# Performance work log

Measured on AMD Instinct MI355X. Metric: run time of the kernel, lower is better.

Reference implementation:

```python
import jax, jax.numpy as jnp
import numpy as np
import math

N_HEADS = 8
TANH_CLIP = 10.0
TEMP = 1.0


def setup_inputs() -> dict:
    key = jax.random.key(0)
    ks = jax.random.split(key, 8)
    B, N, D = 256, 2048, 128
    node_embeddings = jax.random.normal(ks[0], (B, N, D), dtype=jnp.float32)
    W_node = jax.random.normal(ks[1], (D, 3 * D), dtype=jnp.float32) / math.sqrt(D)
    W_fixed = jax.random.normal(ks[2], (D, D), dtype=jnp.float32) / math.sqrt(D)
    W_step = jax.random.normal(ks[3], (2 * D, D), dtype=jnp.float32) / math.sqrt(2 * D)
    W_out = jax.random.normal(ks[4], (D, D), dtype=jnp.float32) / math.sqrt(D)
    first_idx = jax.random.randint(ks[5], (B,), 0, N, dtype=jnp.int32)
    last_idx = jax.random.randint(ks[6], (B,), 0, N, dtype=jnp.int32)
    mask = jax.random.bernoulli(ks[7], 0.5, (B, N))
    mask = mask.at[:, 0].set(False)  # guarantee at least one feasible node per row
    return {"node_embeddings": node_embeddings, "W_node": W_node, "W_fixed": W_fixed,
            "W_step": W_step, "W_out": W_out, "first_idx": first_idx,
            "last_idx": last_idx, "mask": mask}


def reference(node_embeddings, W_node, W_fixed, W_step, W_out, first_idx, last_idx, mask):
    B, N, D = node_embeddings.shape
    H = N_HEADS
    hd = D // H  # key_dim = val_dim = embed_dim / n_heads
    neg_inf = -jnp.inf

    # --- _precompute ---
    graph_embed = node_embeddings.mean(axis=1)                # [B, D]
    fixed_context = graph_embed @ W_fixed                     # [B, D]
    proj = node_embeddings @ W_node                           # [B, N, 3D]
    gK, gV, logit_K = jnp.split(proj, 3, axis=-1)             # each [B, N, D]
    gK = gK.reshape(B, N, H, hd).transpose(2, 0, 1, 3)        # [H, B, N, hd]
    gV = gV.reshape(B, N, H, hd).transpose(2, 0, 1, 3)        # [H, B, N, hd]

    # --- step context: cat(first node emb, last node emb) ---
    first_emb = jnp.take_along_axis(node_embeddings, first_idx[:, None, None].astype(jnp.int32), axis=1)[:, 0]  # [B, D]
    last_emb = jnp.take_along_axis(node_embeddings, last_idx[:, None, None].astype(jnp.int32), axis=1)[:, 0]
    step_ctx = jnp.concatenate([first_emb, last_emb], axis=-1)  # [B, 2D]
    query = fixed_context + step_ctx @ W_step                 # [B, D]

    # --- glimpse multi-head attention (n_query = 1, masked inner) ---
    Q = query.reshape(B, H, hd).transpose(1, 0, 2)            # [H, B, hd]
    compat = jnp.einsum('hbd,hbnd->hbn', Q, gK) / math.sqrt(hd)  # [H, B, N]
    compat = jnp.where(mask[None, :, :], neg_inf, compat)     # mask_inner=True
    attn = jax.nn.softmax(compat, axis=-1)
    heads = jnp.einsum('hbn,hbnd->hbd', attn, gV)             # [H, B, hd]
    glimpse = heads.transpose(1, 0, 2).reshape(B, D) @ W_out  # project_out, [B, D]

    # --- logits with tanh clipping and masking ---
    logits = jnp.einsum('bd,bnd->bn', glimpse, logit_K) / math.sqrt(D)  # [B, N]
    logits = jnp.tanh(logits) * TANH_CLIP
    logits = jnp.where(mask, neg_inf, logits)                 # mask_logits=True
    log_p = jax.nn.log_softmax(logits / TEMP, axis=-1)        # [B, N]
    return log_p
```

## Files before the change

kernel.cpp:

```cpp
#include <hip/hip_runtime.h>
#include <math.h>

#define B_ 256
#define N_ 2048
#define D_ 128
#define NSEG 2048
#define GRID_MEGA 1024

#define NEG_HUGE (-1.0e30f)

#define WSE_BYTES ((size_t)B_ * N_ * D_ * 2)
#define WSQ_OFF 262144
#define WSA_OFF 524288
#define WSB_OFF_M 2654208
#define WSC_OFF_M 2658304
#define BAR_OFF 2691072
#define WS_NEED_BYTES (WSE_BYTES + (size_t)(BAR_OFF + 8) * 4)

#define WSA_STRIDE 1040
#define FB_WSB_OFF (B_ * 8 * WSA_STRIDE)
#define FB_WSC_OFF (FB_WSB_OFF + B_ * 8 * 2)

typedef __attribute__((ext_vector_type(8))) short bf16x8;
typedef __attribute__((ext_vector_type(4))) float f32x4;
typedef __attribute__((ext_vector_type(4))) unsigned short u16x4;
typedef __attribute__((ext_vector_type(2))) int i32x2;

__device__ __forceinline__ float wave_max64(float v) {
#pragma unroll
  for (int off = 32; off > 0; off >>= 1) v = fmaxf(v, __shfl_xor(v, off, 64));
  return v;
}
__device__ __forceinline__ float wave_sum64(float v) {
#pragma unroll
  for (int off = 32; off > 0; off >>= 1) v += __shfl_xor(v, off, 64);
  return v;
}
__device__ __forceinline__ unsigned short bf16rne(float f) {
  unsigned u = __float_as_uint(f);
  u += 0x7FFFu + ((u >> 16) & 1u);
  return (unsigned short)(u >> 16);
}
__device__ __forceinline__ float bflo(unsigned u) { return __uint_as_float(u << 16); }
__device__ __forceinline__ float bfhi(unsigned u) { return __uint_as_float(u & 0xFFFF0000u); }

__device__ __forceinline__ void grid_barrier(unsigned* bar, unsigned nb) {
  __syncthreads();
  if (threadIdx.x == 0) {
    const unsigned mygen = atomicAdd(&bar[1], 0u);
    __threadfence();
    const unsigned arrived = atomicAdd(&bar[0], 1u) + 1u;
    if (arrived == nb) {
      atomicExch(&bar[0], 0u);
      __threadfence();
      atomicAdd(&bar[1], 1u);
    } else {
      while (atomicAdd(&bar[1], 0u) == mygen) { __builtin_amdgcn_s_sleep(8); }
    }
    __threadfence();
  }
  __syncthreads();
}

__global__ void __launch_bounds__(256, 4) k_mega(
    const float* __restrict__ emb, const float* __restrict__ Wnode,
    const float* __restrict__ Wfix, const float* __restrict__ Wstep,
    const float* __restrict__ Wout, const int* __restrict__ fidx,
    const int* __restrict__ lidx, const unsigned char* __restrict__ mask,
    float* __restrict__ buf, unsigned short* __restrict__ wsE,
    float* __restrict__ wsF, unsigned* __restrict__ bar) {
  const int g = blockIdx.x, t = threadIdx.x;
  const unsigned nb = gridDim.x;
  float* wsM = wsF;
  float* wsQ = wsF + WSQ_OFF;
  float* wsA = wsF + WSA_OFF;
  float* wsB = wsF + WSB_OFF_M;
  float* wsC = wsF + WSC_OFF_M;

  __shared__ __align__(16) unsigned char smem[21504];

  for (int seg = g; seg < NSEG; seg += nb) {
    const int b = seg >> 3, s = seg & 7;
    const int f4 = t & 31, gg = t >> 5;
    const size_t rowbase = (size_t)b * N_;
    float4 acc = make_float4(0.f, 0.f, 0.f, 0.f);
    int n = s * 256 + gg;
#pragma unroll 8
    for (int i = 0; i < 32; ++i, n += 8) {
      const float4 v = *(const float4*)(emb + (rowbase + n) * D_ + f4 * 4);
      acc.x += v.x; acc.y += v.y; acc.z += v.z; acc.w += v.w;
      ushort4 o;
      o.x = bf16rne(v.x); o.y = bf16rne(v.y); o.z = bf16rne(v.z); o.w = bf16rne(v.w);
      *(ushort4*)(wsE + (rowbase + n) * D_ + f4 * 4) = o;
    }
    float4* red = (float4*)smem;
    __syncthreads();
    red[t] = acc;
    __syncthreads();
    if (gg == 0) {
      float4 r = red[f4];
#pragma unroll
      for (int j = 1; j < 8; ++j) {
        const float4 a = red[j * 32 + f4];
        r.x += a.x; r.y += a.y; r.z += a.z; r.w += a.w;
      }
      *(float4*)(wsM + (size_t)(b * 8 + s) * 128 + f4 * 4) = r;
    }
  }
  grid_barrier(bar, nb);

  for (int b = g; b < B_; b += nb) {
    float* ge = (float*)smem;
    float* fe = ge + 128;
    float* le = ge + 256;
    float* pq = ge + 384;
    float* q = ge + 640;
    if (t < 128) {
      float ssum = 0.f;
#pragma unroll
      for (int i = 0; i < 8; ++i) ssum += wsM[(size_t)(b * 8 + i) * 128 + t];
      ge[t] = ssum * (1.0f / 2048.0f);
      fe[t] = emb[((size_t)b * N_ + fidx[b]) * D_ + t];
      le[t] = emb[((size_t)b * N_ + lidx[b]) * D_ + t];
    }
    __syncthreads();
    {
      const int j = t & 127, h2 = t >> 7;
      float acc = 0.f;
#pragma unroll 4
      for (int k = 64 * h2; k < 64 * h2 + 64; ++k) {
        acc = fmaf(ge[k], Wfix[k * 128 + j], acc);
        acc = fmaf(fe[k], Wstep[k * 128 + j], acc);
        acc = fmaf(le[k], Wstep[(128 + k) * 128 + j], acc);
      }
      pq[h2 * 128 + j] = acc;
    }
    __syncthreads();
    if (t < 128) q[t] = pq[t] + pq[128 + t];
    __syncthreads();
    if (t < 128) {
      const float* wrow = Wnode + (size_t)t * 384;
#pragma unroll
      for (int h = 0; h < 8; ++h) {
        float a = 0.f;
#pragma unroll
        for (int k = 0; k < 16; ++k) a = fmaf(q[h * 16 + k], wrow[h * 16 + k], a);
        wsQ[(size_t)b * 1024 + h * 128 + t] = a * 0.25f;
      }
    }
    __syncthreads();
  }
  grid_barrier(bar, nb);

  {
    unsigned short* eR = (unsigned short*)smem;
    unsigned short* pT = (unsigned short*)(smem + 18432);
    float* red0 = (float*)(smem + 20736);
    float* red1 = (float*)(smem + 20992);
    float* resc = (float*)(smem + 21248);
    unsigned char* mask_s = smem + 21312;
    const int lane = t & 63, w = t >> 6;
    const int lg = lane >> 4, lc = lane & 15;

    for (int seg = g; seg < NSEG; seg += nb) {
      const int b = seg >> 3, s = seg & 7;
      bf16x8 bq[4];
#pragma unroll
      for (int ks = 0; ks < 4; ++ks)
#pragma unroll
        for (int j = 0; j < 8; ++j) bq[ks][j] = 0;
      if (lc < 8) {
        const float* qrow = wsQ + (size_t)b * 1024 + lc * 128;
#pragma unroll
        for (int ks = 0; ks < 4; ++ks)
#pragma unroll
          for (int j = 0; j < 8; ++j)
            bq[ks][j] = (short)bf16rne(qrow[32 * ks + 8 * lg + j]);
      }

      float m_run = -INFINITY, l_run = 0.f;
      f32x4 wacc0 = {0.f, 0.f, 0.f, 0.f}, wacc1 = {0.f, 0.f, 0.f, 0.f};
      const unsigned short* embB = wsE + ((size_t)b * N_ + s * 256) * D_;
      const unsigned char* mrow = mask + (size_t)b * N_ + s * 256;

      for (int tile = 0; tile < 4; ++tile) {
        __syncthreads();
#pragma unroll
        for (int i = 0; i < 4; ++i) {
          const int gid = t + 256 * i;
          const int n = gid >> 4, d0 = (gid & 15) * 8;
          const int widx =
              ((n >> 2) * 8 + (d0 >> 4)) * 72 + ((n & 3) << 4) + (d0 & 15);
          const uint4 u =
              *(const uint4*)(embB + ((size_t)tile * 64 + n) * D_ + d0);
          *(uint4*)&eR[widx] = u;
        }
        if (t < 64) mask_s[t] = mrow[tile * 64 + t];
        __syncthreads();

        f32x4 sAcc = {0.f, 0.f, 0.f, 0.f};
#pragma unroll
        for (int ks = 0; ks < 4; ++ks) {
          const int aidx = ((4 * w + (lc >> 2)) * 8 + 2 * ks + (lg >> 1)) * 72 +
                           ((lc & 3) << 4) + ((lg & 1) << 3);
          const bf16x8 af = *(const bf16x8*)&eR[aidx];
          sAcc = __builtin_amdgcn_mfma_f32_16x16x32_bf16(af, bq[ks], sAcc, 0, 0, 0);
        }

        float sv[4];
        bool mk[4];
        float tmax = -INFINITY;
#pragma unroll
        for (int r = 0; r < 4; ++r) {
          mk[r] = mask_s[16 * w + 4 * lg + r] != 0;
          sv[r] = mk[r] ? -INFINITY : sAcc[r];
          tmax = fmaxf(tmax, sv[r]);
        }
        tmax = fmaxf(tmax, __shfl_xor(tmax, 16, 64));
        tmax = fmaxf(tmax, __shfl_xor(tmax, 32, 64));
        if (lane < 16) red0[w * 16 + lc] = tmax;
        __syncthreads();

        const float m_tile = fmaxf(fmaxf(red0[lc], red0[16 + lc]),
                                   fmaxf(red0[32 + lc], red0[48 + lc]));
        const float m_new = fmaxf(m_run, m_tile);
        const float rsc = (m_new == -INFINITY) ? 1.f : __expf(m_run - m_new);
        float psum = 0.f;
        unsigned short pu[4];
#pragma unroll
        for (int r = 0; r < 4; ++r) {
          const float p = mk[r] ? 0.f : __expf(sv[r] - m_new);
          psum += p;
          pu[r] = bf16rne(p);
        }
        m_run = m_new;
        psum += __shfl_xor(psum, 16, 64);
        psum += __shfl_xor(psum, 32, 64);
        if (lane < 16) red1[w * 16 + lc] = psum;
        *(u16x4*)&pT[lc * 72 + 16 * w + 4 * lg] = (u16x4){pu[0], pu[1], pu[2], pu[3]};
        if (t < 16) resc[t] = rsc;
        __syncthreads();

        l_run = l_run * rsc +
                (red1[lc] + red1[16 + lc] + red1[32 + lc] + red1[48 + lc]);
        {
          const float r0f = resc[4 * lg + 0], r1f = resc[4 * lg + 1];
          const float r2f = resc[4 * lg + 2], r3f = resc[4 * lg + 3];
          wacc0[0] *= r0f; wacc0[1] *= r1f; wacc0[2] *= r2f; wacc0[3] *= r3f;
          wacc1[0] *= r0f; wacc1[1] *= r1f; wacc1[2] *= r2f; wacc1[3] *= r3f;
        }

        i32x2 tb0a, tb0b, tb1a, tb1b, tb2a, tb2b, tb3a, tb3b;
        {
          const unsigned base00 = (unsigned)(unsigned long long)
              &eR[((0 + 2 * lg) * 8 + w) * 72 + lc];
          const unsigned base01 = (unsigned)(unsigned long long)
              &eR[((0 + 2 * lg) * 8 + (w + 4)) * 72 + lc];
          const unsigned base10 = (unsigned)(unsigned long long)
              &eR[((8 + 2 * lg) * 8 + w) * 72 + lc];
          const unsigned base11 = (unsigned)(unsigned long long)
              &eR[((8 + 2 * lg) * 8 + (w + 4)) * 72 + lc];
          asm volatile("ds_read_b64_tr_b16 %0, %2 offset:0\n\t"
                       "ds_read_b64_tr_b16 %1, %2 offset:1152"
                       : "=v"(tb0a), "=v"(tb0b) : "v"(base00));
          asm volatile("ds_read_b64_tr_b16 %0, %2 offset:0\n\t"
                       "ds_read_b64_tr_b16 %1, %2 offset:1152"
                       : "=v"(tb1a), "=v"(tb1b) : "v"(base01));
          asm volatile("ds_read_b64_tr_b16 %0, %2 offset:0\n\t"
                       "ds_read_b64_tr_b16 %1, %2 offset:1152"
                       : "=v"(tb2a), "=v"(tb2b) : "v"(base10));
          asm volatile("ds_read_b64_tr_b16 %0, %2 offset:0\n\t"
                       "ds_read_b64_tr_b16 %1, %2 offset:1152"
                       : "=v"(tb3a), "=v"(tb3b) : "v"(base11));
          asm volatile("s_waitcnt lgkmcnt(0)" ::: "memory");
          __builtin_amdgcn_sched_barrier(0);
        }
        {
          const bf16x8 pa0 = *(const bf16x8*)&pT[lc * 72 + 8 * lg];
          const bf16x8 pa1 = *(const bf16x8*)&pT[lc * 72 + 32 + 8 * lg];
          union { i32x2 d[2]; bf16x8 v; } u;
          u.d[0] = tb0a; u.d[1] = tb0b;
          wacc0 = __builtin_amdgcn_mfma_f32_16x16x32_bf16(pa0, u.v, wacc0, 0, 0, 0);
          u.d[0] = tb1a; u.d[1] = tb1b;
          wacc1 = __builtin_amdgcn_mfma_f32_16x16x32_bf16(pa0, u.v, wacc1, 0, 0, 0);
          u.d[0] = tb2a; u.d[1] = tb2b;
          wacc0 = __builtin_amdgcn_mfma_f32_16x16x32_bf16(pa1, u.v, wacc0, 0, 0, 0);
          u.d[0] = tb3a; u.d[1] = tb3b;
          wacc1 = __builtin_amdgcn_mfma_f32_16x16x32_bf16(pa1, u.v, wacc1, 0, 0, 0);
        }
        __syncthreads();
      }

      float* dst = wsA + (size_t)(b * 8 + s) * WSA_STRIDE;
      if (lg < 2) {
#pragma unroll
        for (int r = 0; r < 4; ++r) {
          const int h = 4 * lg + r;
          dst[16 + h * 128 + 16 * w + lc] = wacc0[r];
          dst[16 + h * 128 + 16 * (w + 4) + lc] = wacc1[r];
        }
      }
      if (t < 8) { dst[t] = m_run; dst[8 + t] = l_run; }
      __syncthreads();
    }
  }
  grid_barrier(bar, nb);

  for (int b = g; b < B_; b += nb) {
    float* Ls = (float*)smem;
    float* scale = Ls + 8;
    float* wl = scale + 64;
    float* heads = wl + 1024;
    float* glim = heads + 128;
    float* p2 = glim + 128;
    const int j = t & 127, hh = t >> 7;
    const float* base = wsA + (size_t)b * 8 * WSA_STRIDE;

    if (t < 8) {
      float M = -INFINITY;
#pragma unroll
      for (int s = 0; s < 8; ++s) M = fmaxf(M, base[s * WSA_STRIDE + t]);
      float L = 0.f;
#pragma unroll
      for (int s = 0; s < 8; ++s) {
        const float m = base[s * WSA_STRIDE + t];
        const float sc = (m == -INFINITY) ? 0.f : __expf(m - M);
        scale[s * 8 + t] = sc;
        L = fmaf(base[s * WSA_STRIDE + 8 + t], sc, L);
      }
      Ls[t] = L;
    }
    __syncthreads();
#pragma unroll
    for (int k = 0; k < 4; ++k) {
      const int idx = t + 256 * k;
      const int h = idx >> 7, d = idx & 127;
      float acc = 0.f;
#pragma unroll
      for (int s = 0; s < 8; ++s)
        acc = fmaf(scale[s * 8 + h], base[s * WSA_STRIDE + 16 + h * 128 + d], acc);
      wl[idx] = acc;
    }
    __syncthreads();
    {
      const int h = j >> 4, kk = j & 15;
      const float* wp = Wnode + 128 + h * 16 + kk;
      float acc = 0.f;
#pragma unroll 8
      for (int d = 64 * hh; d < 64 * hh + 64; ++d)
        acc = fmaf(wl[h * 128 + d], wp[(size_t)d * 384], acc);
      p2[hh * 128 + j] = acc;
    }
    __syncthreads();
    if (t < 128) heads[t] = (p2[t] + p2[128 + t]) / Ls[t >> 4];
    __syncthreads();
    {
      float acc = 0.f;
#pragma unroll 8
      for (int k = 64 * hh; k < 64 * hh + 64; ++k)
        acc = fmaf(heads[k], Wout[(size_t)k * 128 + j], acc);
      p2[hh * 128 + j] = acc;
    }
    __syncthreads();
    if (t < 128) glim[t] = p2[t] + p2[128 + t];
    __syncthreads();
    {
      const float* wr = Wnode + (size_t)j * 384 + 256;
      float acc = 0.f;
#pragma unroll 8
      for (int k = 64 * hh; k < 64 * hh + 64; ++k) acc = fmaf(wr[k], glim[k], acc);
      p2[hh * 128 + j] = acc;
    }
    __syncthreads();
    if (t < 128)
      wsC[(size_t)b * 128 + t] = (p2[t] + p2[128 + t]) * 0.08838834764831845f;
    __syncthreads();
  }
  grid_barrier(bar, nb);

  {
    float* lgs = (float*)smem;
    const int lane = t & 63, w4 = t >> 6;
    for (int seg = g; seg < NSEG; seg += nb) {
      const int b = seg >> 3, s = seg & 7;
      const float4* c4 = (const float4*)(wsC + (size_t)b * 128);
      const float4 cfa = c4[(t & 15) * 2];
      const float4 cfb = c4[(t & 15) * 2 + 1];
      const unsigned short* embB = wsE + ((size_t)b * N_ + s * 256) * D_;
      const unsigned char* mrow = mask + (size_t)b * N_ + s * 256;
      float mr = NEG_HUGE, sr = 0.f;
      for (int tile = 0; tile < 4; ++tile) {
        const int n0 = tile * 64;
#pragma unroll
        for (int i = 0; i < 4; ++i) {
          const int gid = t + 256 * i;
          const int r = gid >> 4, c8 = (gid & 15) * 8;
          const uint4 u = *(const uint4*)(embB + (size_t)(n0 + r) * D_ + c8);
          float p = bflo(u.x) * cfa.x + bfhi(u.x) * cfa.y;
          p = fmaf(bflo(u.y), cfa.z, p); p = fmaf(bfhi(u.y), cfa.w, p);
          p = fmaf(bflo(u.z), cfb.x, p); p = fmaf(bfhi(u.z), cfb.y, p);
          p = fmaf(bflo(u.w), cfb.z, p); p = fmaf(bfhi(u.w), cfb.w, p);
          p += __shfl_xor(p, 8, 64);
          p += __shfl_xor(p, 4, 64);
          p += __shfl_xor(p, 2, 64);
          p += __shfl_xor(p, 1, 64);
          if ((t & 15) == 0) lgs[r] = p;
        }
        __syncthreads();
        const bool mk = mrow[n0 + lane] != 0;
        const float x = lgs[lane];
        const float ex = __expf(2.f * x);
        const float val = mk ? NEG_HUGE : (10.f - __fdividef(20.f, ex + 1.f));
        const float tm = wave_max64(val);
        const float mn = fmaxf(mr, tm);
        sr = sr * __expf(mr - mn) + wave_sum64(mk ? 0.f : __expf(val - mn));
        mr = mn;
        if (w4 == 0) buf[(size_t)b * N_ + s * 256 + n0 + lane] = val;
        __syncthreads();
      }
      if (t == 0) {
        wsB[(size_t)(b * 8 + s) * 2] = mr;
        wsB[(size_t)(b * 8 + s) * 2 + 1] = sr;
      }
      __syncthreads();
    }
  }
  grid_barrier(bar, nb);

  for (int seg = g; seg < NSEG; seg += nb) {
    const int b = seg >> 3, s = seg & 7;
    float M = NEG_HUGE;
#pragma unroll
    for (int qq = 0; qq < 8; ++qq) M = fmaxf(M, wsB[(size_t)(b * 8 + qq) * 2]);
    float S = 0.f;
#pragma unroll
    for (int qq = 0; qq < 8; ++qq) {
      const float m = wsB[(size_t)(b * 8 + qq) * 2];
      S += wsB[(size_t)(b * 8 + qq) * 2 + 1] * __expf(m - M);
    }
    const float LS = M + logf(S);
    const size_t idx = (size_t)b * N_ + s * 256 + t;
    const float v = buf[idx];
    buf[idx] = (v <= -1.0e29f) ? NEG_HUGE : (v - LS);
  }
}

__global__ void __launch_bounds__(256) k_prep(const float* __restrict__ emb,
                                              float* __restrict__ buf) {
  const int b = blockIdx.x, s = blockIdx.y, t = threadIdx.x;
  const int f4 = t & 31, g = t >> 5;
  const size_t rowbase = (size_t)b * N_;
  float4 acc = make_float4(0.f, 0.f, 0.f, 0.f);
  int n = s * 256 + g;
#pragma unroll 8
  for (int i = 0; i < 32; ++i, n += 8) {
    const float4 v = *(const float4*)(emb + (rowbase + n) * D_ + f4 * 4);
    acc.x += v.x; acc.y += v.y; acc.z += v.z; acc.w += v.w;
  }
  __shared__ float4 red[256];
  red[t] = acc;
  __syncthreads();
  if (g == 0) {
    float4 r = red[f4];
#pragma unroll
    for (int j = 1; j < 8; ++j) {
      const float4 a = red[j * 32 + f4];
      r.x += a.x; r.y += a.y; r.z += a.z; r.w += a.w;
    }
    *(float4*)(buf + (size_t)b * N_ + s * 128 + f4 * 4) = r;
  }
}

__global__ void __launch_bounds__(384) k_query(const float* __restrict__ emb,
                                               const float* __restrict__ Wfix,
                                               const float* __restrict__ Wstep,
                                               const float* __restrict__ Wnode,
                                               const int* __restrict__ fidx,
                                               const int* __restrict__ lidx,
                                               float* __restrict__ buf) {
  const int b = blockIdx.x, t = threadIdx.x;
  __shared__ float x[384];
  __shared__ float part[3][128];
  __shared__ float q[128];
  if (t < 128) {
    float ssum = 0.f;
#pragma unroll
    for (int i = 0; i < 8; ++i) ssum += buf[(size_t)b * N_ + i * 128 + t];
    x[t] = ssum * (1.0f / 2048.0f);
  } else if (t < 256) {
    x[t] = emb[((size_t)b * N_ + fidx[b]) * D_ + (t - 128)];
  } else {
    x[t] = emb[((size_t)b * N_ + lidx[b]) * D_ + (t - 256)];
  }
  __syncthreads();
  {
    const int seg = t >> 7, j = t & 127;
    const float* xs = &x[seg * 128];
    const float* Wp = (seg == 0) ? (Wfix + j) : (Wstep + (seg == 1 ? 0 : 128 * 128) + j);
    float acc = 0.f;
#pragma unroll 8
    for (int k = 0; k < 128; ++k) acc = fmaf(xs[k], Wp[(size_t)k * 128], acc);
    part[seg][j] = acc;
  }
  __syncthreads();
  if (t < 128) q[t] = part[0][t] + part[1][t] + part[2][t];
  __syncthreads();
  if (t < 128) {
    const float* wrow = Wnode + (size_t)t * 384;
#pragma unroll
    for (int h = 0; h < 8; ++h) {
      float a = 0.f;
#pragma unroll
      for (int k = 0; k < 16; ++k) a = fmaf(q[h * 16 + k], wrow[h * 16 + k], a);
      buf[(size_t)b * N_ + 1024 + h * 128 + t] = a * 0.25f;
    }
  }
}

__global__ void __launch_bounds__(256) k_attn_m(const float* __restrict__ emb,
                                                const unsigned char* __restrict__ mask,
                                                const float* __restrict__ buf,
                                                float* __restrict__ wsA) {
  const int b = blockIdx.x, s = blockIdx.y;
  const int t = threadIdx.x;
  const int lane = t & 63, w = t >> 6;
  const int lg = lane >> 4, lc = lane & 15;
  __shared__ __align__(16) unsigned short eR[9216];
  __shared__ __align__(16) unsigned short pT[16 * 72];
  __shared__ float red0[4][16];
  __shared__ float red1[4][16];
  __shared__ float resc_s[16];
  __shared__ unsigned char mask_s[64];
  bf16x8 bq[4];
#pragma unroll
  for (int ks = 0; ks < 4; ++ks)
#pragma unroll
    for (int j = 0; j < 8; ++j) bq[ks][j] = 0;
  if (lc < 8) {
    const float* qrow = buf + (size_t)b * N_ + 1024 + lc * 128;
#pragma unroll
    for (int ks = 0; ks < 4; ++ks)
#pragma unroll
      for (int j = 0; j < 8; ++j)
        bq[ks][j] = (short)bf16rne(qrow[32 * ks + 8 * lg + j]);
  }
  float m_run = -INFINITY, l_run = 0.f;
  f32x4 wacc0 = {0.f, 0.f, 0.f, 0.f}, wacc1 = {0.f, 0.f, 0.f, 0.f};
  const float* embb = emb + ((size_t)b * N_ + s * 256) * D_;
  const unsigned char* mrow = mask + (size_t)b * N_ + s * 256;
  for (int tile = 0; tile < 4; ++tile) {
    {
      const float* src = embb + (size_t)tile * 64 * D_;
#pragma unroll
      for (int i = 0; i < 4; ++i) {
        const int gid = t + 256 * i;
        const int n = gid >> 4, d0 = (gid & 15) * 8;
        const float4 v0 = *(const float4*)(src + (size_t)n * D_ + d0);
        const float4 v1 = *(const float4*)(src + (size_t)n * D_ + d0 + 4);
        bf16x8 ev;
        ev[0] = (short)bf16rne(v0.x); ev[1] = (short)bf16rne(v0.y);
        ev[2] = (short)bf16rne(v0.z); ev[3] = (short)bf16rne(v0.w);
        ev[4] = (short)bf16rne(v1.x); ev[5] = (short)bf16rne(v1.y);
        ev[6] = (short)bf16rne(v1.z); ev[7] = (short)bf16rne(v1.w);
        const int widx = ((n >> 2) * 8 + (d0 >> 4)) * 72 + ((n & 3) << 4) + (d0 & 15);
        *(bf16x8*)&eR[widx] = ev;
      }
      if (t < 64) mask_s[t] = mrow[tile * 64 + t];
    }
    __syncthreads();
    f32x4 sAcc = {0.f, 0.f, 0.f, 0.f};
#pragma unroll
    for (int ks = 0; ks < 4; ++ks) {
      const int aidx = ((4 * w + (lc >> 2)) * 8 + 2 * ks + (lg >> 1)) * 72 +
                       ((lc & 3) << 4) + ((lg & 1) << 3);
      const bf16x8 af = *(const bf16x8*)&eR[aidx];
      sAcc = __builtin_amdgcn_mfma_f32_16x16x32_bf16(af, bq[ks], sAcc, 0, 0, 0);
    }
    float sv[4];
    bool mk[4];
    float tmax = -INFINITY;
#pragma unroll
    for (int r = 0; r < 4; ++r) {
      mk[r] = mask_s[16 * w + 4 * lg + r] != 0;
      sv[r] = mk[r] ? -INFINITY : sAcc[r];
      tmax = fmaxf(tmax, sv[r]);
    }
    tmax = fmaxf(tmax, __shfl_xor(tmax, 16, 64));
    tmax = fmaxf(tmax, __shfl_xor(tmax, 32, 64));
    if (lane < 16) red0[w][lc] = tmax;
    __syncthreads();
    const float m_tile = fmaxf(fmaxf(red0[0][lc], red0[1][lc]),
                               fmaxf(red0[2][lc], red0[3][lc]));
    const float m_new = fmaxf(m_run, m_tile);
    const float rsc = (m_new == -INFINITY) ? 1.f : __expf(m_run - m_new);
    float psum = 0.f;
    unsigned short pu[4];
#pragma unroll
    for (int r = 0; r < 4; ++r) {
      const float p = mk[r] ? 0.f : __expf(sv[r] - m_new);
      psum += p;
      pu[r] = bf16rne(p);
    }
    m_run = m_new;
    psum += __shfl_xor(psum, 16, 64);
    psum += __shfl_xor(psum, 32, 64);
    if (lane < 16) red1[w][lc] = psum;
    *(u16x4*)&pT[lc * 72 + 16 * w + 4 * lg] = (u16x4){pu[0], pu[1], pu[2], pu[3]};
    if (t < 16) resc_s[t] = rsc;
    __syncthreads();
    l_run = l_run * rsc + (red1[0][lc] + red1[1][lc] + red1[2][lc] + red1[3][lc]);
    {
      const float r0f = resc_s[4 * lg + 0], r1f = resc_s[4 * lg + 1];
      const float r2f = resc_s[4 * lg + 2], r3f = resc_s[4 * lg + 3];
      wacc0[0] *= r0f; wacc0[1] *= r1f; wacc0[2] *= r2f; wacc0[3] *= r3f;
      wacc1[0] *= r0f; wacc1[1] *= r1f; wacc1[2] *= r2f; wacc1[3] *= r3f;
    }
    i32x2 tb0a, tb0b, tb1a, tb1b, tb2a, tb2b, tb3a, tb3b;
    {
      const unsigned base00 = (unsigned)(unsigned long long)
          &eR[((0 + 2 * lg) * 8 + w) * 72 + lc];
      const unsigned base01 = (unsigned)(unsigned long long)
          &eR[((0 + 2 * lg) * 8 + (w + 4)) * 72 + lc];
      const unsigned base10 = (unsigned)(unsigned long long)
          &eR[((8 + 2 * lg) * 8 + w) * 72 + lc];
      const unsigned base11 = (unsigned)(unsigned long long)
          &eR[((8 + 2 * lg) * 8 + (w + 4)) * 72 + lc];
      asm volatile("ds_read_b64_tr_b16 %0, %2 offset:0\n\t"
                   "ds_read_b64_tr_b16 %1, %2 offset:1152"
                   : "=v"(tb0a), "=v"(tb0b) : "v"(base00));
      asm volatile("ds_read_b64_tr_b16 %0, %2 offset:0\n\t"
                   "ds_read_b64_tr_b16 %1, %2 offset:1152"
                   : "=v"(tb1a), "=v"(tb1b) : "v"(base01));
      asm volatile("ds_read_b64_tr_b16 %0, %2 offset:0\n\t"
                   "ds_read_b64_tr_b16 %1, %2 offset:1152"
                   : "=v"(tb2a), "=v"(tb2b) : "v"(base10));
      asm volatile("ds_read_b64_tr_b16 %0, %2 offset:0\n\t"
                   "ds_read_b64_tr_b16 %1, %2 offset:1152"
                   : "=v"(tb3a), "=v"(tb3b) : "v"(base11));
      asm volatile("s_waitcnt lgkmcnt(0)" ::: "memory");
      __builtin_amdgcn_sched_barrier(0);
    }
    {
      const bf16x8 pa0 = *(const bf16x8*)&pT[lc * 72 + 8 * lg];
      const bf16x8 pa1 = *(const bf16x8*)&pT[lc * 72 + 32 + 8 * lg];
      union { i32x2 d[2]; bf16x8 v; } u;
      u.d[0] = tb0a; u.d[1] = tb0b;
      wacc0 = __builtin_amdgcn_mfma_f32_16x16x32_bf16(pa0, u.v, wacc0, 0, 0, 0);
      u.d[0] = tb1a; u.d[1] = tb1b;
      wacc1 = __builtin_amdgcn_mfma_f32_16x16x32_bf16(pa0, u.v, wacc1, 0, 0, 0);
      u.d[0] = tb2a; u.d[1] = tb2b;
      wacc0 = __builtin_amdgcn_mfma_f32_16x16x32_bf16(pa1, u.v, wacc0, 0, 0, 0);
      u.d[0] = tb3a; u.d[1] = tb3b;
      wacc1 = __builtin_amdgcn_mfma_f32_16x16x32_bf16(pa1, u.v, wacc1, 0, 0, 0);
    }
    __syncthreads();
  }
  float* dst = wsA + (size_t)(b * 8 + s) * WSA_STRIDE;
  if (lg < 2) {
#pragma unroll
    for (int r = 0; r < 4; ++r) {
      const int h = 4 * lg + r;
      dst[16 + h * 128 + 16 * w + lc] = wacc0[r];
      dst[16 + h * 128 + 16 * (w + 4) + lc] = wacc1[r];
    }
  }
  if (t < 8) { dst[t] = m_run; dst[8 + t] = l_run; }
}

__global__ void __launch_bounds__(256) k_attn_comb(const float* __restrict__ Wnode,
                                                   const float* __restrict__ Wout,
                                                   const float* __restrict__ wsA,
                                                   float* __restrict__ wsC) {
  const int b = blockIdx.x, t = threadIdx.x;
  const int j = t & 127, hh = t >> 7;
  const float* base = wsA + (size_t)b * 8 * WSA_STRIDE;
  __shared__ float Ls[8], scale[8][8];
  __shared__ float wl[8 * 128], heads[128], glim[128];
  __shared__ float part2[2][128];
  if (t < 8) {
    float M = -INFINITY;
#pragma unroll
    for (int s = 0; s < 8; ++s) M = fmaxf(M, base[s * WSA_STRIDE + t]);
    float L = 0.f;
#pragma unroll
    for (int s = 0; s < 8; ++s) {
      const float m = base[s * WSA_STRIDE + t];
      const float sc = (m == -INFINITY) ? 0.f : __expf(m - M);
      scale[s][t] = sc;
      L = fmaf(base[s * WSA_STRIDE + 8 + t], sc, L);
    }
    Ls[t] = L;
  }
  __syncthreads();
#pragma unroll
  for (int k = 0; k < 4; ++k) {
    const int idx = t + 256 * k;
    const int h = idx >> 7, d = idx & 127;
    float acc = 0.f;
#pragma unroll
    for (int s = 0; s < 8; ++s)
      acc = fmaf(scale[s][h], base[s * WSA_STRIDE + 16 + h * 128 + d], acc);
    wl[idx] = acc;
  }
  __syncthreads();
  {
    const int h = j >> 4, kk = j & 15;
    const float* wp = Wnode + 128 + h * 16 + kk;
    float acc = 0.f;
#pragma unroll 8
    for (int d = 64 * hh; d < 64 * hh + 64; ++d)
      acc = fmaf(wl[h * 128 + d], wp[(size_t)d * 384], acc);
    part2[hh][j] = acc;
  }
  __syncthreads();
  if (t < 128) heads[t] = (part2[0][t] + part2[1][t]) / Ls[t >> 4];
  __syncthreads();
  {
    float acc = 0.f;
#pragma unroll 8
    for (int k = 64 * hh; k < 64 * hh + 64; ++k)
      acc = fmaf(heads[k], Wout[(size_t)k * 128 + j], acc);
    part2[hh][j] = acc;
  }
  __syncthreads();
  if (t < 128) glim[t] = part2[0][t] + part2[1][t];
  __syncthreads();
  {
    const float* wr = Wnode + (size_t)j * 384 + 256;
    float acc = 0.f;
#pragma unroll 8
    for (int k = 64 * hh; k < 64 * hh + 64; ++k) acc = fmaf(wr[k], glim[k], acc);
    part2[hh][j] = acc;
  }
  __syncthreads();
  if (t < 128)
    wsC[(size_t)b * 128 + t] = (part2[0][t] + part2[1][t]) * 0.08838834764831845f;
}

__global__ void __launch_bounds__(256) k_logits_part(const float* __restrict__ emb,
                                                     const unsigned char* __restrict__ mask,
                                                     const float* __restrict__ wsC,
                                                     float* __restrict__ buf,
                                                     float* __restrict__ wsB) {
  const int b = blockIdx.x, s = blockIdx.y;
  const int t = threadIdx.x, lane = t & 63, w = t >> 6;
  __shared__ float lg[64];
  const float4 cf = ((const float4*)(wsC + (size_t)b * 128))[t & 31];
  const float* embb = emb + ((size_t)b * N_ + s * 256) * D_;
  const unsigned char* mrow = mask + (size_t)b * N_ + s * 256;
  float mr = NEG_HUGE, sr = 0.f;
  for (int tile = 0; tile < 4; ++tile) {
    const int n0 = tile * 64;
#pragma unroll
    for (int i = 0; i < 8; ++i) {
      const int gid = t + 256 * i;
      const int r = gid >> 5, c = (gid & 31) * 4;
      const float4 e = *(const float4*)(embb + (size_t)(n0 + r) * D_ + c);
      float p = fmaf(e.x, cf.x, fmaf(e.y, cf.y, fmaf(e.z, cf.z, e.w * cf.w)));
      p += __shfl_xor(p, 16, 64);
      p += __shfl_xor(p, 8, 64);
      p += __shfl_xor(p, 4, 64);
      p += __shfl_xor(p, 2, 64);
      p += __shfl_xor(p, 1, 64);
      if ((t & 31) == 0) lg[r] = p;
    }
    __syncthreads();
    const bool mk = mrow[n0 + lane] != 0;
    const float x = lg[lane];
    const float ex = __expf(2.f * x);
    const float val = mk ? NEG_HUGE : (10.f - __fdividef(20.f, ex + 1.f));
    const float tm = wave_max64(val);
    const float mn = fmaxf(mr, tm);
    sr = sr * __expf(mr - mn) + wave_sum64(mk ? 0.f : __expf(val - mn));
    mr = mn;
    if (w == 0) buf[(size_t)b * N_ + s * 256 + n0 + lane] = val;
    __syncthreads();
  }
  if (t == 0) {
    wsB[(size_t)(b * 8 + s) * 2] = mr;
    wsB[(size_t)(b * 8 + s) * 2 + 1] = sr;
  }
}

__global__ void __launch_bounds__(256) k_norm(const float* __restrict__ wsB,
                                              float* __restrict__ buf) {
  const int b = blockIdx.x, s = blockIdx.y, t = threadIdx.x;
  float M = NEG_HUGE;
#pragma unroll
  for (int q = 0; q < 8; ++q) M = fmaxf(M, wsB[(size_t)(b * 8 + q) * 2]);
  float S = 0.f;
#pragma unroll
  for (int q = 0; q < 8; ++q) {
    const float m = wsB[(size_t)(b * 8 + q) * 2];
    S += wsB[(size_t)(b * 8 + q) * 2 + 1] * __expf(m - M);
  }
  const float LS = M + logf(S);
  const size_t idx = (size_t)b * N_ + s * 256 + t;
  const float v = buf[idx];
  buf[idx] = (v <= -1.0e29f) ? NEG_HUGE : (v - LS);
}

extern "C" void kernel_launch(void* const* d_in, const int* in_sizes, int n_in,
                              void* d_out, int out_size, void* d_ws, size_t ws_size,
                              hipStream_t stream) {
  (void)in_sizes; (void)n_in; (void)out_size;
  const float* emb = (const float*)d_in[0];
  const float* Wnode = (const float*)d_in[1];
  const float* Wfix = (const float*)d_in[2];
  const float* Wstep = (const float*)d_in[3];
  const float* Wout = (const float*)d_in[4];
  const int* fidx = (const int*)d_in[5];
  const int* lidx = (const int*)d_in[6];
  const unsigned char* mask = (const unsigned char*)d_in[7];
  float* buf = (float*)d_out;

  int occ = 0;
  (void)hipOccupancyMaxActiveBlocksPerMultiprocessor(&occ, k_mega, 256, 0);

  if (occ >= 4 && ws_size >= WS_NEED_BYTES) {
    unsigned short* wsE = (unsigned short*)d_ws;
    float* wsF = (float*)((char*)d_ws + WSE_BYTES);
    unsigned* bar = (unsigned*)(wsF + BAR_OFF);
    hipMemsetAsync(bar, 0, 8, stream);
    k_mega<<<GRID_MEGA, 256, 0, stream>>>(emb, Wnode, Wfix, Wstep, Wout, fidx,
                                          lidx, mask, buf, wsE, wsF, bar);
  } else {
    float* ws = (float*)d_ws;
    k_prep<<<dim3(B_, 8), 256, 0, stream>>>(emb, buf);
    k_query<<<B_, 384, 0, stream>>>(emb, Wfix, Wstep, Wnode, fidx, lidx, buf);
    k_attn_m<<<dim3(B_, 8), 256, 0, stream>>>(emb, mask, buf, ws);
    k_attn_comb<<<B_, 256, 0, stream>>>(Wnode, Wout, ws, ws + FB_WSC_OFF);
    k_logits_part<<<dim3(B_, 8), 256, 0, stream>>>(emb, mask, ws + FB_WSC_OFF, buf,
                                                   ws + FB_WSB_OFF);
    k_norm<<<dim3(B_, 8), 256, 0, stream>>>(ws + FB_WSB_OFF, buf);
  }
}
```

Baseline: 160.2 us.

## Replace grid-wide barriers with per-batch dataflow flags in persistent kernel

The persistent megakernel's five global grid barriers are replaced by a dataflow scheme (k_flow) in which per-batch-row flag counters in workspace signal when each stage's partial results are ready. Blocks can then move on to later stages for rows whose inputs are complete instead of waiting for the whole grid. Stage bodies are split into device helper functions shared with the fallback path. In exchange, this adds flag polling and memory-fence traffic, and it risks deadlock or ordering bugs if blocks are not all co-resident or if work is assigned in an order that leaves some flags unsatisfied.

```diff
diff --git a/kernel.cpp b/kernel.cpp
--- a/kernel.cpp
+++ b/kernel.cpp
@@ -4,8 +4,7 @@
 #define B_ 256
 #define N_ 2048
 #define D_ 128
-#define NSEG 2048
-#define GRID_MEGA 1024
+#define GRID_F 1024
 
 #define NEG_HUGE (-1.0e30f)
 
@@ -14,8 +13,8 @@
 #define WSA_OFF 524288
 #define WSB_OFF_M 2654208
 #define WSC_OFF_M 2658304
-#define BAR_OFF 2691072
-#define WS_NEED_BYTES (WSE_BYTES + (size_t)(BAR_OFF + 8) * 4)
+#define FLAGS_OFF 2691072
+#define WS_NEED_BYTES (WSE_BYTES + (size_t)(FLAGS_OFF + 1280) * 4)
 
 #define WSA_STRIDE 1040
 #define FB_WSB_OFF (B_ * 8 * WSA_STRIDE)
@@ -44,466 +43,73 @@
 __device__ __forceinline__ float bflo(unsigned u) { return __uint_as_float(u << 16); }
 __device__ __forceinline__ float bfhi(unsigned u) { return __uint_as_float(u & 0xFFFF0000u); }
 
-__device__ __forceinline__ void grid_barrier(unsigned* bar, unsigned nb) {
-  __syncthreads();
-  if (threadIdx.x == 0) {
-    const unsigned mygen = atomicAdd(&bar[1], 0u);
-    __threadfence();
-    const unsigned arrived = atomicAdd(&bar[0], 1u) + 1u;
-    if (arrived == nb) {
-      atomicExch(&bar[0], 0u);
-      __threadfence();
-      atomicAdd(&bar[1], 1u);
-    } else {
-      while (atomicAdd(&bar[1], 0u) == mygen) { __builtin_amdgcn_s_sleep(8); }
-    }
-    __threadfence();
-  }
-  __syncthreads();
-}
-
-__global__ void __launch_bounds__(256, 4) k_mega(
-    const float* __restrict__ emb, const float* __restrict__ Wnode,
-    const float* __restrict__ Wfix, const float* __restrict__ Wstep,
-    const float* __restrict__ Wout, const int* __restrict__ fidx,
-    const int* __restrict__ lidx, const unsigned char* __restrict__ mask,
-    float* __restrict__ buf, unsigned short* __restrict__ wsE,
-    float* __restrict__ wsF, unsigned* __restrict__ bar) {
-  const int g = blockIdx.x, t = threadIdx.x;
-  const unsigned nb = gridDim.x;
-  float* wsM = wsF;
-  float* wsQ = wsF + WSQ_OFF;
-  float* wsA = wsF + WSA_OFF;
-  float* wsB = wsF + WSB_OFF_M;
-  float* wsC = wsF + WSC_OFF_M;
-
-  __shared__ __align__(16) unsigned char smem[21504];
-
-  for (int seg = g; seg < NSEG; seg += nb) {
-    const int b = seg >> 3, s = seg & 7;
-    const int f4 = t & 31, gg = t >> 5;
-    const size_t rowbase = (size_t)b * N_;
-    float4 acc = make_float4(0.f, 0.f, 0.f, 0.f);
-    int n = s * 256 + gg;
-#pragma unroll 8
-    for (int i = 0; i < 32; ++i, n += 8) {
-      const float4 v = *(const float4*)(emb + (rowbase + n) * D_ + f4 * 4);
-      acc.x += v.x; acc.y += v.y; acc.z += v.z; acc.w += v.w;
-      ushort4 o;
-      o.x = bf16rne(v.x); o.y = bf16rne(v.y); o.z = bf16rne(v.z); o.w = bf16rne(v.w);
-      *(ushort4*)(wsE + (rowbase + n) * D_ + f4 * 4) = o;
-    }
-    float4* red = (float4*)smem;
-    __syncthreads();
-    red[t] = acc;
-    __syncthreads();
-    if (gg == 0) {
-      float4 r = red[f4];
-#pragma unroll
-      for (int j = 1; j < 8; ++j) {
-        const float4 a = red[j * 32 + f4];
-        r.x += a.x; r.y += a.y; r.z += a.z; r.w += a.w;
-      }
-      *(float4*)(wsM + (size_t)(b * 8 + s) * 128 + f4 * 4) = r;
-    }
-  }
-  grid_barrier(bar, nb);
-
-  for (int b = g; b < B_; b += nb) {
-    float* ge = (float*)smem;
-    float* fe = ge + 128;
-    float* le = ge + 256;
-    float* pq = ge + 384;
-    float* q = ge + 640;
-    if (t < 128) {
-      float ssum = 0.f;
-#pragma unroll
-      for (int i = 0; i < 8; ++i) ssum += wsM[(size_t)(b * 8 + i) * 128 + t];
-      ge[t] = ssum * (1.0f / 2048.0f);
-      fe[t] = emb[((size_t)b * N_ + fidx[b]) * D_ + t];
-      le[t] = emb[((size_t)b * N_ + lidx[b]) * D_ + t];
-    }
-    __syncthreads();
-    {
-      const int j = t & 127, h2 = t >> 7;
-      float acc = 0.f;
-#pragma unroll 4
-      for (int k = 64 * h2; k < 64 * h2 + 64; ++k) {
-        acc = fmaf(ge[k], Wfix[k * 128 + j], acc);
-        acc = fmaf(fe[k], Wstep[k * 128 + j], acc);
-        acc = fmaf(le[k], Wstep[(128 + k) * 128 + j], acc);
-      }
-      pq[h2 * 128 + j] = acc;
-    }
-    __syncthreads();
-    if (t < 128) q[t] = pq[t] + pq[128 + t];
-    __syncthreads();
-    if (t < 128) {
-      const float* wrow = Wnode + (size_t)t * 384;
-#pragma unroll
-      for (int h = 0; h < 8; ++h) {
-        float a = 0.f;
-#pragma unroll
-        for (int k = 0; k < 16; ++k) a = fmaf(q[h * 16 + k], wrow[h * 16 + k], a);
-        wsQ[(size_t)b * 1024 + h * 128 + t] = a * 0.25f;
-      }
-    }
-    __syncthreads();
-  }
-  grid_barrier(bar, nb);
-
-  {
-    unsigned short* eR = (unsigned short*)smem;
-    unsigned short* pT = (unsigned short*)(smem + 18432);
-    float* red0 = (float*)(smem + 20736);
-    float* red1 = (float*)(smem + 20992);
-    float* resc = (float*)(smem + 21248);
-    unsigned char* mask_s = smem + 21312;
-    const int lane = t & 63, w = t >> 6;
-    const int lg = lane >> 4, lc = lane & 15;
-
-    for (int seg = g; seg < NSEG; seg += nb) {
-      const int b = seg >> 3, s = seg & 7;
-      bf16x8 bq[4];
-#pragma unroll
-      for (int ks = 0; ks < 4; ++ks)
-#pragma unroll
-        for (int j = 0; j < 8; ++j) bq[ks][j] = 0;
-      if (lc < 8) {
-        const float* qrow = wsQ + (size_t)b * 1024 + lc * 128;
-#pragma unroll
-        for (int ks = 0; ks < 4; ++ks)
-#pragma unroll
-          for (int j = 0; j < 8; ++j)
-            bq[ks][j] = (short)bf16rne(qrow[32 * ks + 8 * lg + j]);
-      }
-
-      float m_run = -INFINITY, l_run = 0.f;
-      f32x4 wacc0 = {0.f, 0.f, 0.f, 0.f}, wacc1 = {0.f, 0.f, 0.f, 0.f};
-      const unsigned short* embB = wsE + ((size_t)b * N_ + s * 256) * D_;
-      const unsigned char* mrow = mask + (size_t)b * N_ + s * 256;
-
-      for (int tile = 0; tile < 4; ++tile) {
-        __syncthreads();
-#pragma unroll
-        for (int i = 0; i < 4; ++i) {
-          const int gid = t + 256 * i;
-          const int n = gid >> 4, d0 = (gid & 15) * 8;
-          const int widx =
-              ((n >> 2) * 8 + (d0 >> 4)) * 72 + ((n & 3) << 4) + (d0 & 15);
-          const uint4 u =
-              *(const uint4*)(embB + ((size_t)tile * 64 + n) * D_ + d0);
-          *(uint4*)&eR[widx] = u;
-        }
-        if (t < 64) mask_s[t] = mrow[tile * 64 + t];
-        __syncthreads();
-
-        f32x4 sAcc = {0.f, 0.f, 0.f, 0.f};
-#pragma unroll
-        for (int ks = 0; ks < 4; ++ks) {
-          const int aidx = ((4 * w + (lc >> 2)) * 8 + 2 * ks + (lg >> 1)) * 72 +
-                           ((lc & 3) << 4) + ((lg & 1) << 3);
-          const bf16x8 af = *(const bf16x8*)&eR[aidx];
-          sAcc = __builtin_amdgcn_mfma_f32_16x16x32_bf16(af, bq[ks], sAcc, 0, 0, 0);
-        }
-
-        float sv[4];
-        bool mk[4];
-        float tmax = -INFINITY;
-#pragma unroll
-        for (int r = 0; r < 4; ++r) {
-          mk[r] = mask_s[16 * w + 4 * lg + r] != 0;
-          sv[r] = mk[r] ? -INFINITY : sAcc[r];
-          tmax = fmaxf(tmax, sv[r]);
-        }
-        tmax = fmaxf(tmax, __shfl_xor(tmax, 16, 64));
-        tmax = fmaxf(tmax, __shfl_xor(tmax, 32, 64));
-        if (lane < 16) red0[w * 16 + lc] = tmax;
-        __syncthreads();
-
-        const float m_tile = fmaxf(fmaxf(red0[lc], red0[16 + lc]),
-                                   fmaxf(red0[32 + lc], red0[48 + lc]));
-        const float m_new = fmaxf(m_run, m_tile);
-        const float rsc = (m_new == -INFINITY) ? 1.f : __expf(m_run - m_new);
-        float psum = 0.f;
-        unsigned short pu[4];
-#pragma unroll
-        for (int r = 0; r < 4; ++r) {
-          const float p = mk[r] ? 0.f : __expf(sv[r] - m_new);
-          psum += p;
-          pu[r] = bf16rne(p);
-        }
-        m_run = m_new;
-        psum += __shfl_xor(psum, 16, 64);
-        psum += __shfl_xor(psum, 32, 64);
-        if (lane < 16) red1[w * 16 + lc] = psum;
-        *(u16x4*)&pT[lc * 72 + 16 * w + 4 * lg] = (u16x4){pu[0], pu[1], pu[2], pu[3]};
-        if (t < 16) resc[t] = rsc;
-        __syncthreads();
-
-        l_run = l_run * rsc +
-                (red1[lc] + red1[16 + lc] + red1[32 + lc] + red1[48 + lc]);
-        {
-          const float r0f = resc[4 * lg + 0], r1f = resc[4 * lg + 1];
-          const float r2f = resc[4 * lg + 2], r3f = resc[4 * lg + 3];
-          wacc0[0] *= r0f; wacc0[1] *= r1f; wacc0[2] *= r2f; wacc0[3] *= r3f;
-          wacc1[0] *= r0f; wacc1[1] *= r1f; wacc1[2] *= r2f; wacc1[3] *= r3f;
-        }
-
-        i32x2 tb0a, tb0b, tb1a, tb1b, tb2a, tb2b, tb3a, tb3b;
-        {
-          const unsigned base00 = (unsigned)(unsigned long long)
-              &eR[((0 + 2 * lg) * 8 + w) * 72 + lc];
-          const unsigned base01 = (unsigned)(unsigned long long)
-              &eR[((0 + 2 * lg) * 8 + (w + 4)) * 72 + lc];
-          const unsigned base10 = (unsigned)(unsigned long long)
-              &eR[((8 + 2 * lg) * 8 + w) * 72 + lc];
-          const unsigned base11 = (unsigned)(unsigned long long)
-              &eR[((8 + 2 * lg) * 8 + (w + 4)) * 72 + lc];
-          asm volatile("ds_read_b64_tr_b16 %0, %2 offset:0\n\t"
-                       "ds_read_b64_tr_b16 %1, %2 offset:1152"
-                       : "=v"(tb0a), "=v"(tb0b) : "v"(base00));
-          asm volatile("ds_read_b64_tr_b16 %0, %2 offset:0\n\t"
-                       "ds_read_b64_tr_b16 %1, %2 offset:1152"
-                       : "=v"(tb1a), "=v"(tb1b) : "v"(base01));
-          asm volatile("ds_read_b64_tr_b16 %0, %2 offset:0\n\t"
-                       "ds_read_b64_tr_b16 %1, %2 offset:1152"
-                       : "=v"(tb2a), "=v"(tb2b) : "v"(base10));
-          asm volatile("ds_read_b64_tr_b16 %0, %2 offset:0\n\t"
-                       "ds_read_b64_tr_b16 %1, %2 offset:1152"
-                       : "=v"(tb3a), "=v"(tb3b) : "v"(base11));
-          asm volatile("s_waitcnt lgkmcnt(0)" ::: "memory");
-          __builtin_amdgcn_sched_barrier(0);
-        }
-        {
-          const bf16x8 pa0 = *(const bf16x8*)&pT[lc * 72 + 8 * lg];
-          const bf16x8 pa1 = *(const bf16x8*)&pT[lc * 72 + 32 + 8 * lg];
-          union { i32x2 d[2]; bf16x8 v; } u;
-          u.d[0] = tb0a; u.d[1] = tb0b;
-          wacc0 = __builtin_amdgcn_mfma_f32_16x16x32_bf16(pa0, u.v, wacc0, 0, 0, 0);
-          u.d[0] = tb1a; u.d[1] = tb1b;
-          wacc1 = __builtin_amdgcn_mfma_f32_16x16x32_bf16(pa0, u.v, wacc1, 0, 0, 0);
-          u.d[0] = tb2a; u.d[1] = tb2b;
-          wacc0 = __builtin_amdgcn_mfma_f32_16x16x32_bf16(pa1, u.v, wacc0, 0, 0, 0);
-          u.d[0] = tb3a; u.d[1] = tb3b;
-          wacc1 = __builtin_amdgcn_mfma_f32_16x16x32_bf16(pa1, u.v, wacc1, 0, 0, 0);
-        }
-        __syncthreads();
-      }
-
-      float* dst = wsA + (size_t)(b * 8 + s) * WSA_STRIDE;
-      if (lg < 2) {
-#pragma unroll
-        for (int r = 0; r < 4; ++r) {
-          const int h = 4 * lg + r;
-          dst[16 + h * 128 + 16 * w + lc] = wacc0[r];
-          dst[16 + h * 128 + 16 * (w + 4) + lc] = wacc1[r];
-        }
-      }
-      if (t < 8) { dst[t] = m_run; dst[8 + t] = l_run; }
-      __syncthreads();
-    }
-  }
-  grid_barrier(bar, nb);
-
-  for (int b = g; b < B_; b += nb) {
-    float* Ls = (float*)smem;
-    float* scale = Ls + 8;
-    float* wl = scale + 64;
-    float* heads = wl + 1024;
-    float* glim = heads + 128;
-    float* p2 = glim + 128;
-    const int j = t & 127, hh = t >> 7;
-    const float* base = wsA + (size_t)b * 8 * WSA_STRIDE;
-
-    if (t < 8) {
-      float M = -INFINITY;
-#pragma unroll
-      for (int s = 0; s < 8; ++s) M = fmaxf(M, base[s * WSA_STRIDE + t]);
-      float L = 0.f;
-#pragma unroll
-      for (int s = 0; s < 8; ++s) {
-        const float m = base[s * WSA_STRIDE + t];
-        const float sc = (m == -INFINITY) ? 0.f : __expf(m - M);
-        scale[s * 8 + t] = sc;
-        L = fmaf(base[s * WSA_STRIDE + 8 + t], sc, L);
-      }
-      Ls[t] = L;
-    }
-    __syncthreads();
-#pragma unroll
-    for (int k = 0; k < 4; ++k) {
-      const int idx = t + 256 * k;
-      const int h = idx >> 7, d = idx & 127;
-      float acc = 0.f;
-#pragma unroll
-      for (int s = 0; s < 8; ++s)
-        acc = fmaf(scale[s * 8 + h], base[s * WSA_STRIDE + 16 + h * 128 + d], acc);
-      wl[idx] = acc;
-    }
-    __syncthreads();
-    {
-      const int h = j >> 4, kk = j & 15;
-      const float* wp = Wnode + 128 + h * 16 + kk;
-      float acc = 0.f;
-#pragma unroll 8
-      for (int d = 64 * hh; d < 64 * hh + 64; ++d)
-        acc = fmaf(wl[h * 128 + d], wp[(size_t)d * 384], acc);
-      p2[hh * 128 + j] = acc;
-    }
-    __syncthreads();
-    if (t < 128) heads[t] = (p2[t] + p2[128 + t]) / Ls[t >> 4];
-    __syncthreads();
-    {
-      float acc = 0.f;
-#pragma unroll 8
-      for (int k = 64 * hh; k < 64 * hh + 64; ++k)
-        acc = fmaf(heads[k], Wout[(size_t)k * 128 + j], acc);
-      p2[hh * 128 + j] = acc;
-    }
-    __syncthreads();
-    if (t < 128) glim[t] = p2[t] + p2[128 + t];
-    __syncthreads();
-    {
-      const float* wr = Wnode + (size_t)j * 384 + 256;
-      float acc = 0.f;
-#pragma unroll 8
-      for (int k = 64 * hh; k < 64 * hh + 64; ++k) acc = fmaf(wr[k], glim[k], acc);
-      p2[hh * 128 + j] = acc;
-    }
-    __syncthreads();
-    if (t < 128)
-      wsC[(size_t)b * 128 + t] = (p2[t] + p2[128 + t]) * 0.08838834764831845f;
-    __syncthreads();
-  }
-  grid_barrier(bar, nb);
-
-  {
-    float* lgs = (float*)smem;
-    const int lane = t & 63, w4 = t >> 6;
-    for (int seg = g; seg < NSEG; seg += nb) {
-      const int b = seg >> 3, s = seg & 7;
-      const float4* c4 = (const float4*)(wsC + (size_t)b * 128);
-      const float4 cfa = c4[(t & 15) * 2];
-      const float4 cfb = c4[(t & 15) * 2 + 1];
-      const unsigned short* embB = wsE + ((size_t)b * N_ + s * 256) * D_;
-      const unsigned char* mrow = mask + (size_t)b * N_ + s * 256;
-      float mr = NEG_HUGE, sr = 0.f;
-      for (int tile = 0; tile < 4; ++tile) {
-        const int n0 = tile * 64;
-#pragma unroll
-        for (int i = 0; i < 4; ++i) {
-          const int gid = t + 256 * i;
-          const int r = gid >> 4, c8 = (gid & 15) * 8;
-          const uint4 u = *(const uint4*)(embB + (size_t)(n0 + r) * D_ + c8);
-          float p = bflo(u.x) * cfa.x + bfhi(u.x) * cfa.y;
-          p = fmaf(bflo(u.y), cfa.z, p); p = fmaf(bfhi(u.y), cfa.w, p);
-          p = fmaf(bflo(u.z), cfb.x, p); p = fmaf(bfhi(u.z), cfb.y, p);
-          p = fmaf(bflo(u.w), cfb.z, p); p = fmaf(bfhi(u.w), cfb.w, p);
-          p += __shfl_xor(p, 8, 64);
-          p += __shfl_xor(p, 4, 64);
-          p += __shfl_xor(p, 2, 64);
-          p += __shfl_xor(p, 1, 64);
-          if ((t & 15) == 0) lgs[r] = p;
-        }
-        __syncthreads();
-        const bool mk = mrow[n0 + lane] != 0;
-        const float x = lgs[lane];
-        const float ex = __expf(2.f * x);
-        const float val = mk ? NEG_HUGE : (10.f - __fdividef(20.f, ex + 1.f));
-        const float tm = wave_max64(val);
-        const float mn = fmaxf(mr, tm);
-        sr = sr * __expf(mr - mn) + wave_sum64(mk ? 0.f : __expf(val - mn));
-        mr = mn;
-        if (w4 == 0) buf[(size_t)b * N_ + s * 256 + n0 + lane] = val;
-        __syncthreads();
-      }
-      if (t == 0) {
-        wsB[(size_t)(b * 8 + s) * 2] = mr;
-        wsB[(size_t)(b * 8 + s) * 2 + 1] = sr;
-      }
-      __syncthreads();
-    }
-  }
-  grid_barrier(bar, nb);
-
-  for (int seg = g; seg < NSEG; seg += nb) {
-    const int b = seg >> 3, s = seg & 7;
-    float M = NEG_HUGE;
-#pragma unroll
-    for (int qq = 0; qq < 8; ++qq) M = fmaxf(M, wsB[(size_t)(b * 8 + qq) * 2]);
-    float S = 0.f;
-#pragma unroll
-    for (int qq = 0; qq < 8; ++qq) {
-      const float m = wsB[(size_t)(b * 8 + qq) * 2];
-      S += wsB[(size_t)(b * 8 + qq) * 2 + 1] * __expf(m - M);
-    }
-    const float LS = M + logf(S);
-    const size_t idx = (size_t)b * N_ + s * 256 + t;
-    const float v = buf[idx];
-    buf[idx] = (v <= -1.0e29f) ? NEG_HUGE : (v - LS);
-  }
-}
-
-__global__ void __launch_bounds__(256) k_prep(const float* __restrict__ emb,
-                                              float* __restrict__ buf) {
-  const int b = blockIdx.x, s = blockIdx.y, t = threadIdx.x;
-  const int f4 = t & 31, g = t >> 5;
+__device__ __forceinline__ void do_A(const float* __restrict__ emb,
+                                     unsigned short* __restrict__ wsE,
+                                     float* __restrict__ wsM, int b, int s, int t,
+                                     unsigned char* smem) {
+  const int f4 = t & 31, gg = t >> 5;
   const size_t rowbase = (size_t)b * N_;
   float4 acc = make_float4(0.f, 0.f, 0.f, 0.f);
-  int n = s * 256 + g;
+  int n = s * 256 + gg;
 #pragma unroll 8
   for (int i = 0; i < 32; ++i, n += 8) {
     const float4 v = *(const float4*)(emb + (rowbase + n) * D_ + f4 * 4);
     acc.x += v.x; acc.y += v.y; acc.z += v.z; acc.w += v.w;
-  }
-  __shared__ float4 red[256];
+    ushort4 o;
+    o.x = bf16rne(v.x); o.y = bf16rne(v.y); o.z = bf16rne(v.z); o.w = bf16rne(v.w);
+    *(ushort4*)(wsE + (rowbase + n) * D_ + f4 * 4) = o;
+  }
+  float4* red = (float4*)smem;
+  __syncthreads();
   red[t] = acc;
   __syncthreads();
-  if (g == 0) {
+  if (gg == 0) {
     float4 r = red[f4];
 #pragma unroll
     for (int j = 1; j < 8; ++j) {
       const float4 a = red[j * 32 + f4];
       r.x += a.x; r.y += a.y; r.z += a.z; r.w += a.w;
     }
-    *(float4*)(buf + (size_t)b * N_ + s * 128 + f4 * 4) = r;
-  }
-}
-
-__global__ void __launch_bounds__(384) k_query(const float* __restrict__ emb,
-                                               const float* __restrict__ Wfix,
-                                               const float* __restrict__ Wstep,
-                                               const float* __restrict__ Wnode,
-                                               const int* __restrict__ fidx,
-                                               const int* __restrict__ lidx,
-                                               float* __restrict__ buf) {
-  const int b = blockIdx.x, t = threadIdx.x;
-  __shared__ float x[384];
-  __shared__ float part[3][128];
-  __shared__ float q[128];
+    *(float4*)(wsM + (size_t)(b * 8 + s) * 128 + f4 * 4) = r;
+  }
+}
+
+__device__ __forceinline__ void do_B(const float* __restrict__ emb,
+                                     const float* __restrict__ Wfix,
+                                     const float* __restrict__ Wstep,
+                                     const float* __restrict__ Wnode,
+                                     const int* __restrict__ fidx,
+                                     const int* __restrict__ lidx,
+                                     const float* __restrict__ wsM,
+                                     float* __restrict__ wsQ, int b, int t,
+                                     unsigned char* smem) {
+  float* ge = (float*)smem;
+  float* fe = ge + 128;
+  float* le = ge + 256;
+  float* pq = ge + 384;
+  float* q = ge + 640;
   if (t < 128) {
     float ssum = 0.f;
 #pragma unroll
-    for (int i = 0; i < 8; ++i) ssum += buf[(size_t)b * N_ + i * 128 + t];
-    x[t] = ssum * (1.0f / 2048.0f);
-  } else if (t < 256) {
-    x[t] = emb[((size_t)b * N_ + fidx[b]) * D_ + (t - 128)];
-  } else {
-    x[t] = emb[((size_t)b * N_ + lidx[b]) * D_ + (t - 256)];
+    for (int i = 0; i < 8; ++i) ssum += wsM[(size_t)(b * 8 + i) * 128 + t];
+    ge[t] = ssum * (1.0f / 2048.0f);
+    fe[t] = emb[((size_t)b * N_ + fidx[b]) * D_ + t];
+    le[t] = emb[((size_t)b * N_ + lidx[b]) * D_ + t];
   }
   __syncthreads();
   {
-    const int seg = t >> 7, j = t & 127;
-    const float* xs = &x[seg * 128];
-    const float* Wp = (seg == 0) ? (Wfix + j) : (Wstep + (seg == 1 ? 0 : 128 * 128) + j);
+    const int j = t & 127, h2 = t >> 7;
     float acc = 0.f;
-#pragma unroll 8
-    for (int k = 0; k < 128; ++k) acc = fmaf(xs[k], Wp[(size_t)k * 128], acc);
-    part[seg][j] = acc;
-  }
-  __syncthreads();
-  if (t < 128) q[t] = part[0][t] + part[1][t] + part[2][t];
+#pragma unroll 4
+    for (int k = 64 * h2; k < 64 * h2 + 64; ++k) {
+      acc = fmaf(ge[k], Wfix[k * 128 + j], acc);
+      acc = fmaf(fe[k], Wstep[k * 128 + j], acc);
+      acc = fmaf(le[k], Wstep[(128 + k) * 128 + j], acc);
+    }
+    pq[h2 * 128 + j] = acc;
+  }
+  __syncthreads();
+  if (t < 128) q[t] = pq[t] + pq[128 + t];
   __syncthreads();
   if (t < 128) {
     const float* wrow = Wnode + (size_t)t * 384;
@@ -512,62 +118,57 @@
       float a = 0.f;
 #pragma unroll
       for (int k = 0; k < 16; ++k) a = fmaf(q[h * 16 + k], wrow[h * 16 + k], a);
-      buf[(size_t)b * N_ + 1024 + h * 128 + t] = a * 0.25f;
-    }
-  }
-}
-
-__global__ void __launch_bounds__(256) k_attn_m(const float* __restrict__ emb,
-                                                const unsigned char* __restrict__ mask,
-                                                const float* __restrict__ buf,
-                                                float* __restrict__ wsA) {
-  const int b = blockIdx.x, s = blockIdx.y;
-  const int t = threadIdx.x;
+      wsQ[(size_t)b * 1024 + h * 128 + t] = a * 0.25f;
+    }
+  }
+}
+
+__device__ __forceinline__ void do_C(const unsigned short* __restrict__ wsE,
+                                     const unsigned char* __restrict__ mask,
+                                     const float* __restrict__ wsQ,
+                                     float* __restrict__ wsA, int b, int s, int t,
+                                     unsigned char* smem) {
+  unsigned short* eR = (unsigned short*)smem;
+  unsigned short* pT = (unsigned short*)(smem + 18432);
+  float* red0 = (float*)(smem + 20736);
+  float* red1 = (float*)(smem + 20992);
+  float* resc = (float*)(smem + 21248);
+  unsigned char* mask_s = smem + 21312;
   const int lane = t & 63, w = t >> 6;
   const int lg = lane >> 4, lc = lane & 15;
-  __shared__ __align__(16) unsigned short eR[9216];
-  __shared__ __align__(16) unsigned short pT[16 * 72];
-  __shared__ float red0[4][16];
-  __shared__ float red1[4][16];
-  __shared__ float resc_s[16];
-  __shared__ unsigned char mask_s[64];
+
   bf16x8 bq[4];
 #pragma unroll
   for (int ks = 0; ks < 4; ++ks)
 #pragma unroll
     for (int j = 0; j < 8; ++j) bq[ks][j] = 0;
   if (lc < 8) {
-    const float* qrow = buf + (size_t)b * N_ + 1024 + lc * 128;
+    const float* qrow = wsQ + (size_t)b * 1024 + lc * 128;
 #pragma unroll
     for (int ks = 0; ks < 4; ++ks)
 #pragma unroll
       for (int j = 0; j < 8; ++j)
         bq[ks][j] = (short)bf16rne(qrow[32 * ks + 8 * lg + j]);
   }
+
   float m_run = -INFINITY, l_run = 0.f;
   f32x4 wacc0 = {0.f, 0.f, 0.f, 0.f}, wacc1 = {0.f, 0.f, 0.f, 0.f};
-  const float* embb = emb + ((size_t)b * N_ + s * 256) * D_;
+  const unsigned short* embB = wsE + ((size_t)b * N_ + s * 256) * D_;
   const unsigned char* mrow = mask + (size_t)b * N_ + s * 256;
+
   for (int tile = 0; tile < 4; ++tile) {
-    {
-      const float* src = embb + (size_t)tile * 64 * D_;
-#pragma unroll
-      for (int i = 0; i < 4; ++i) {
-        const int gid = t + 256 * i;
-        const int n = gid >> 4, d0 = (gid & 15) * 8;
-        const float4 v0 = *(const float4*)(src + (size_t)n * D_ + d0);
-        const float4 v1 = *(const float4*)(src + (size_t)n * D_ + d0 + 4);
-        bf16x8 ev;
-        ev[0] = (short)bf16rne(v0.x); ev[1] = (short)bf16rne(v0.y);
-        ev[2] = (short)bf16rne(v0.z); ev[3] = (short)bf16rne(v0.w);
-        ev[4] = (short)bf16rne(v1.x); ev[5] = (short)bf16rne(v1.y);
-        ev[6] = (short)bf16rne(v1.z); ev[7] = (short)bf16rne(v1.w);
-        const int widx = ((n >> 2) * 8 + (d0 >> 4)) * 72 + ((n & 3) << 4) + (d0 & 15);
-        *(bf16x8*)&eR[widx] = ev;
-      }
-      if (t < 64) mask_s[t] = mrow[tile * 64 + t];
-    }
-    __syncthreads();
+    __syncthreads();
+#pragma unroll
+    for (int i = 0; i < 4; ++i) {
+      const int gid = t + 256 * i;
+      const int n = gid >> 4, d0 = (gid & 15) * 8;
+      const int widx = ((n >> 2) * 8 + (d0 >> 4)) * 72 + ((n & 3) << 4) + (d0 & 15);
+      const uint4 u = *(const uint4*)(embB + ((size_t)tile * 64 + n) * D_ + d0);
+      *(uint4*)&eR[widx] = u;
+    }
+    if (t < 64) mask_s[t] = mrow[tile * 64 + t];
+    __syncthreads();
+
     f32x4 sAcc = {0.f, 0.f, 0.f, 0.f};
 #pragma unroll
     for (int ks = 0; ks < 4; ++ks) {
@@ -576,6 +177,7 @@
       const bf16x8 af = *(const bf16x8*)&eR[aidx];
       sAcc = __builtin_amdgcn_mfma_f32_16x16x32_bf16(af, bq[ks], sAcc, 0, 0, 0);
     }
+
     float sv[4];
     bool mk[4];
     float tmax = -INFINITY;
@@ -587,10 +189,11 @@
     }
     tmax = fmaxf(tmax, __shfl_xor(tmax, 16, 64));
     tmax = fmaxf(tmax, __shfl_xor(tmax, 32, 64));
-    if (lane < 16) red0[w][lc] = tmax;
-    __syncthreads();
-    const float m_tile = fmaxf(fmaxf(red0[0][lc], red0[1][lc]),
-                               fmaxf(red0[2][lc], red0[3][lc]));
+    if (lane < 16) red0[w * 16 + lc] = tmax;
+    __syncthreads();
+
+    const float m_tile = fmaxf(fmaxf(red0[lc], red0[16 + lc]),
+                               fmaxf(red0[32 + lc], red0[48 + lc]));
     const float m_new = fmaxf(m_run, m_tile);
     const float rsc = (m_new == -INFINITY) ? 1.f : __expf(m_run - m_new);
     float psum = 0.f;
@@ -604,17 +207,19 @@
     m_run = m_new;
     psum += __shfl_xor(psum, 16, 64);
     psum += __shfl_xor(psum, 32, 64);
-    if (lane < 16) red1[w][lc] = psum;
+    if (lane < 16) red1[w * 16 + lc] = psum;
     *(u16x4*)&pT[lc * 72 + 16 * w + 4 * lg] = (u16x4){pu[0], pu[1], pu[2], pu[3]};
-    if (t < 16) resc_s[t] = rsc;
-    __syncthreads();
-    l_run = l_run * rsc + (red1[0][lc] + red1[1][lc] + red1[2][lc] + red1[3][lc]);
+    if (t < 16) resc[t] = rsc;
+    __syncthreads();
+
+    l_run = l_run * rsc + (red1[lc] + red1[16 + lc] + red1[32 + lc] + red1[48 + lc]);
     {
-      const float r0f = resc_s[4 * lg + 0], r1f = resc_s[4 * lg + 1];
-      const float r2f = resc_s[4 * lg + 2], r3f = resc_s[4 * lg + 3];
+      const float r0f = resc[4 * lg + 0], r1f = resc[4 * lg + 1];
+      const float r2f = resc[4 * lg + 2], r3f = resc[4 * lg + 3];
       wacc0[0] *= r0f; wacc0[1] *= r1f; wacc0[2] *= r2f; wacc0[3] *= r3f;
       wacc1[0] *= r0f; wacc1[1] *= r1f; wacc1[2] *= r2f; wacc1[3] *= r3f;
     }
+
     i32x2 tb0a, tb0b, tb1a, tb1b, tb2a, tb2b, tb3a, tb3b;
     {
       const unsigned base00 = (unsigned)(unsigned long long)
@@ -655,6 +260,7 @@
     }
     __syncthreads();
   }
+
   float* dst = wsA + (size_t)(b * 8 + s) * WSA_STRIDE;
   if (lg < 2) {
 #pragma unroll
@@ -667,16 +273,20 @@
   if (t < 8) { dst[t] = m_run; dst[8 + t] = l_run; }
 }
 
-__global__ void __launch_bounds__(256) k_attn_comb(const float* __restrict__ Wnode,
-                                                   const float* __restrict__ Wout,
-                                                   const float* __restrict__ wsA,
-                                                   float* __restrict__ wsC) {
-  const int b = blockIdx.x, t = threadIdx.x;
+__device__ __forceinline__ void do_D(const float* __restrict__ Wnode,
+                                     const float* __restrict__ Wout,
+                                     const float* __restrict__ wsA,
+                                     float* __restrict__ wsC, int b, int t,
+                                     unsigned char* smem) {
+  float* Ls = (float*)smem;
+  float* scale = Ls + 8;
+  float* wl = scale + 64;
+  float* heads = wl + 1024;
+  float* glim = heads + 128;
+  float* p2 = glim + 128;
   const int j = t & 127, hh = t >> 7;
   const float* base = wsA + (size_t)b * 8 * WSA_STRIDE;
-  __shared__ float Ls[8], scale[8][8];
-  __shared__ float wl[8 * 128], heads[128], glim[128];
-  __shared__ float part2[2][128];
+
   if (t < 8) {
     float M = -INFINITY;
 #pragma unroll
@@ -686,7 +296,7 @@
     for (int s = 0; s < 8; ++s) {
       const float m = base[s * WSA_STRIDE + t];
       const float sc = (m == -INFINITY) ? 0.f : __expf(m - M);
-      scale[s][t] = sc;
+      scale[s * 8 + t] = sc;
       L = fmaf(base[s * WSA_STRIDE + 8 + t], sc, L);
     }
     Ls[t] = L;
@@ -699,7 +309,7 @@
     float acc = 0.f;
 #pragma unroll
     for (int s = 0; s < 8; ++s)
-      acc = fmaf(scale[s][h], base[s * WSA_STRIDE + 16 + h * 128 + d], acc);
+      acc = fmaf(scale[s * 8 + h], base[s * WSA_STRIDE + 16 + h * 128 + d], acc);
     wl[idx] = acc;
   }
   __syncthreads();
@@ -710,31 +320,397 @@
 #pragma unroll 8
     for (int d = 64 * hh; d < 64 * hh + 64; ++d)
       acc = fmaf(wl[h * 128 + d], wp[(size_t)d * 384], acc);
-    part2[hh][j] = acc;
-  }
-  __syncthreads();
-  if (t < 128) heads[t] = (part2[0][t] + part2[1][t]) / Ls[t >> 4];
+    p2[hh * 128 + j] = acc;
+  }
+  __syncthreads();
+  if (t < 128) heads[t] = (p2[t] + p2[128 + t]) / Ls[t >> 4];
   __syncthreads();
   {
     float acc = 0.f;
 #pragma unroll 8
     for (int k = 64 * hh; k < 64 * hh + 64; ++k)
       acc = fmaf(heads[k], Wout[(size_t)k * 128 + j], acc);
-    part2[hh][j] = acc;
-  }
-  __syncthreads();
-  if (t < 128) glim[t] = part2[0][t] + part2[1][t];
+    p2[hh * 128 + j] = acc;
+  }
+  __syncthreads();
+  if (t < 128) glim[t] = p2[t] + p2[128 + t];
   __syncthreads();
   {
     const float* wr = Wnode + (size_t)j * 384 + 256;
     float acc = 0.f;
 #pragma unroll 8
     for (int k = 64 * hh; k < 64 * hh + 64; ++k) acc = fmaf(wr[k], glim[k], acc);
-    part2[hh][j] = acc;
+    p2[hh * 128 + j] = acc;
   }
   __syncthreads();
   if (t < 128)
-    wsC[(size_t)b * 128 + t] = (part2[0][t] + part2[1][t]) * 0.08838834764831845f;
+    wsC[(size_t)b * 128 + t] = (p2[t] + p2[128 + t]) * 0.08838834764831845f;
+}
+
+__device__ __forceinline__ void do_E(const unsigned short* __restrict__ wsE,
+                                     const unsigned char* __restrict__ mask,
+                                     const float* __restrict__ wsC,
+                                     float* __restrict__ buf,
+                                     float* __restrict__ wsB, int b, int s, int t,
+                                     unsigned char* smem) {
+  float* lgs = (float*)smem;
+  const int lane = t & 63, w4 = t >> 6;
+  const float4* c4 = (const float4*)(wsC + (size_t)b * 128);
+  const float4 cfa = c4[(t & 15) * 2];
+  const float4 cfb = c4[(t & 15) * 2 + 1];
+  const unsigned short* embB = wsE + ((size_t)b * N_ + s * 256) * D_;
+  const unsigned char* mrow = mask + (size_t)b * N_ + s * 256;
+  float mr = NEG_HUGE, sr = 0.f;
+  for (int tile = 0; tile < 4; ++tile) {
+    const int n0 = tile * 64;
+#pragma unroll
+    for (int i = 0; i < 4; ++i) {
+      const int gid = t + 256 * i;
+      const int r = gid >> 4, c8 = (gid & 15) * 8;
+      const uint4 u = *(const uint4*)(embB + (size_t)(n0 + r) * D_ + c8);
+      float p = bflo(u.x) * cfa.x + bfhi(u.x) * cfa.y;
+      p = fmaf(bflo(u.y), cfa.z, p); p = fmaf(bfhi(u.y), cfa.w, p);
+      p = fmaf(bflo(u.z), cfb.x, p); p = fmaf(bfhi(u.z), cfb.y, p);
+      p = fmaf(bflo(u.w), cfb.z, p); p = fmaf(bfhi(u.w), cfb.w, p);
+      p += __shfl_xor(p, 8, 64);
+      p += __shfl_xor(p, 4, 64);
+      p += __shfl_xor(p, 2, 64);
+      p += __shfl_xor(p, 1, 64);
+      if ((t & 15) == 0) lgs[r] = p;
+    }
+    __syncthreads();
+    const bool mk = mrow[n0 + lane] != 0;
+    const float x = lgs[lane];
+    const float ex = __expf(2.f * x);
+    const float val = mk ? NEG_HUGE : (10.f - __fdividef(20.f, ex + 1.f));
+    const float tm = wave_max64(val);
+    const float mn = fmaxf(mr, tm);
+    sr = sr * __expf(mr - mn) + wave_sum64(mk ? 0.f : __expf(val - mn));
+    mr = mn;
+    if (w4 == 0) buf[(size_t)b * N_ + s * 256 + n0 + lane] = val;
+    __syncthreads();
+  }
+  if (t == 0) {
+    wsB[(size_t)(b * 8 + s) * 2] = mr;
+    wsB[(size_t)(b * 8 + s) * 2 + 1] = sr;
+  }
+}
+
+__device__ __forceinline__ void do_F(const float* __restrict__ wsB,
+                                     float* __restrict__ buf, int b, int t) {
+  float M = NEG_HUGE;
+#pragma unroll
+  for (int q = 0; q < 8; ++q) M = fmaxf(M, wsB[(size_t)(b * 8 + q) * 2]);
+  float S = 0.f;
+#pragma unroll
+  for (int q = 0; q < 8; ++q) {
+    const float m = wsB[(size_t)(b * 8 + q) * 2];
+    S += wsB[(size_t)(b * 8 + q) * 2 + 1] * __expf(m - M);
+  }
+  const float LS = M + logf(S);
+#pragma unroll
+  for (int i = 0; i < 8; ++i) {
+    const size_t idx = (size_t)b * N_ + i * 256 + t;
+    const float v = buf[idx];
+    buf[idx] = (v <= -1.0e29f) ? NEG_HUGE : (v - LS);
+  }
+}
+
+__global__ void __launch_bounds__(256, 4) k_flow(
+    const float* __restrict__ emb, const float* __restrict__ Wnode,
+    const float* __restrict__ Wfix, const float* __restrict__ Wstep,
+    const float* __restrict__ Wout, const int* __restrict__ fidx,
+    const int* __restrict__ lidx, const unsigned char* __restrict__ mask,
+    float* __restrict__ buf, unsigned short* __restrict__ wsE,
+    float* __restrict__ wsF, unsigned* __restrict__ flg) {
+  const int g = blockIdx.x, t = threadIdx.x;
+  float* wsM = wsF;
+  float* wsQ = wsF + WSQ_OFF;
+  float* wsA = wsF + WSA_OFF;
+  float* wsB = wsF + WSB_OFF_M;
+  float* wsC = wsF + WSC_OFF_M;
+  unsigned* aprog = flg;
+  unsigned* qrdy = flg + 256;
+  unsigned* cprog = flg + 512;
+  unsigned* crdy = flg + 768;
+  unsigned* eprog = flg + 1024;
+
+  __shared__ __align__(16) unsigned char smem[21504];
+  __shared__ unsigned sh_old;
+
+#pragma unroll 1
+  for (int pass = 0; pass < 2; ++pass) {
+    const int seg = g + GRID_F * pass;
+    const int b = seg >> 3, s = seg & 7;
+
+    do_A(emb, wsE, wsM, b, s, t, smem);
+    __syncthreads();
+    if (t == 0) { __threadfence(); sh_old = atomicAdd(&aprog[b], 1u); }
+    __syncthreads();
+    if (sh_old == 7u) {
+      do_B(emb, Wfix, Wstep, Wnode, fidx, lidx, wsM, wsQ, b, t, smem);
+      __syncthreads();
+      if (t == 0) { __threadfence(); atomicExch(&qrdy[b], 1u); }
+    }
+
+    if (t == 0) {
+      while (atomicAdd(&qrdy[b], 0u) == 0u) __builtin_amdgcn_s_sleep(8);
+      __threadfence();
+    }
+    __syncthreads();
+    do_C(wsE, mask, wsQ, wsA, b, s, t, smem);
+    __syncthreads();
+    if (t == 0) { __threadfence(); sh_old = atomicAdd(&cprog[b], 1u); }
+    __syncthreads();
+    if (sh_old == 7u) {
+      do_D(Wnode, Wout, wsA, wsC, b, t, smem);
+      __syncthreads();
+      if (t == 0) { __threadfence(); atomicExch(&crdy[b], 1u); }
+    }
+
+    if (t == 0) {
+      while (atomicAdd(&crdy[b], 0u) == 0u) __builtin_amdgcn_s_sleep(8);
+      __threadfence();
+    }
+    __syncthreads();
+    do_E(wsE, mask, wsC, buf, wsB, b, s, t, smem);
+    __syncthreads();
+    if (t == 0) { __threadfence(); sh_old = atomicAdd(&eprog[b], 1u); }
+    __syncthreads();
+    if (sh_old == 7u) do_F(wsB, buf, b, t);
+    __syncthreads();
+  }
+}
+
+__global__ void __launch_bounds__(256) k_prep(const float* __restrict__ emb,
+                                              float* __restrict__ buf) {
+  const int b = blockIdx.x, s = blockIdx.y, t = threadIdx.x;
+  const int f4 = t & 31, g = t >> 5;
+  const size_t rowbase = (size_t)b * N_;
+  float4 acc = make_float4(0.f, 0.f, 0.f, 0.f);
+  int n = s * 256 + g;
+#pragma unroll 8
+  for (int i = 0; i < 32; ++i, n += 8) {
+    const float4 v = *(const float4*)(emb + (rowbase + n) * D_ + f4 * 4);
+    acc.x += v.x; acc.y += v.y; acc.z += v.z; acc.w += v.w;
+  }
+  __shared__ float4 red[256];
+  red[t] = acc;
+  __syncthreads();
+  if (g == 0) {
+    float4 r = red[f4];
+#pragma unroll
+    for (int j = 1; j < 8; ++j) {
+      const float4 a = red[j * 32 + f4];
+      r.x += a.x; r.y += a.y; r.z += a.z; r.w += a.w;
+    }
+    *(float4*)(buf + (size_t)b * N_ + s * 128 + f4 * 4) = r;
+  }
+}
+
+__global__ void __launch_bounds__(384) k_query(const float* __restrict__ emb,
+                                               const float* __restrict__ Wfix,
+                                               const float* __restrict__ Wstep,
+                                               const float* __restrict__ Wnode,
+                                               const int* __restrict__ fidx,
+                                               const int* __restrict__ lidx,
+                                               float* __restrict__ buf) {
+  const int b = blockIdx.x, t = threadIdx.x;
+  __shared__ float x[384];
+  __shared__ float part[3][128];
+  __shared__ float q[128];
+  if (t < 128) {
+    float ssum = 0.f;
+#pragma unroll
+    for (int i = 0; i < 8; ++i) ssum += buf[(size_t)b * N_ + i * 128 + t];
+    x[t] = ssum * (1.0f / 2048.0f);
+  } else if (t < 256) {
+    x[t] = emb[((size_t)b * N_ + fidx[b]) * D_ + (t - 128)];
+  } else {
+    x[t] = emb[((size_t)b * N_ + lidx[b]) * D_ + (t - 256)];
+  }
+  __syncthreads();
+  {
+    const int seg = t >> 7, j = t & 127;
+    const float* xs = &x[seg * 128];
+    const float* Wp = (seg == 0) ? (Wfix + j) : (Wstep + (seg == 1 ? 0 : 128 * 128) + j);
+    float acc = 0.f;
+#pragma unroll 8
+    for (int k = 0; k < 128; ++k) acc = fmaf(xs[k], Wp[(size_t)k * 128], acc);
+    part[seg][j] = acc;
+  }
+  __syncthreads();
+  if (t < 128) q[t] = part[0][t] + part[1][t] + part[2][t];
+  __syncthreads();
+  if (t < 128) {
+    const float* wrow = Wnode + (size_t)t * 384;
+#pragma unroll
+    for (int h = 0; h < 8; ++h) {
+      float a = 0.f;
+#pragma unroll
+      for (int k = 0; k < 16; ++k) a = fmaf(q[h * 16 + k], wrow[h * 16 + k], a);
+      buf[(size_t)b * N_ + 1024 + h * 128 + t] = a * 0.25f;
+    }
+  }
+}
+
+__global__ void __launch_bounds__(256) k_attn_m(const float* __restrict__ emb,
+                                                const unsigned char* __restrict__ mask,
+                                                const float* __restrict__ buf,
+                                                float* __restrict__ wsA) {
+  const int b = blockIdx.x, s = blockIdx.y;
+  const int t = threadIdx.x;
+  const int lane = t & 63, w = t >> 6;
+  const int lg = lane >> 4, lc = lane & 15;
+  __shared__ __align__(16) unsigned char smem[21504];
+  unsigned short* eR = (unsigned short*)smem;
+  bf16x8 bq[4];
+#pragma unroll
+  for (int ks = 0; ks < 4; ++ks)
+#pragma unroll
+    for (int j = 0; j < 8; ++j) bq[ks][j] = 0;
+  if (lc < 8) {
+    const float* qrow = buf + (size_t)b * N_ + 1024 + lc * 128;
+#pragma unroll
+    for (int ks = 0; ks < 4; ++ks)
+#pragma unroll
+      for (int j = 0; j < 8; ++j)
+        bq[ks][j] = (short)bf16rne(qrow[32 * ks + 8 * lg + j]);
+  }
+  unsigned short* pT = (unsigned short*)(smem + 18432);
+  float* red0 = (float*)(smem + 20736);
+  float* red1 = (float*)(smem + 20992);
+  float* resc = (float*)(smem + 21248);
+  unsigned char* mask_s = smem + 21312;
+  float m_run = -INFINITY, l_run = 0.f;
+  f32x4 wacc0 = {0.f, 0.f, 0.f, 0.f}, wacc1 = {0.f, 0.f, 0.f, 0.f};
+  const float* embb = emb + ((size_t)b * N_ + s * 256) * D_;
+  const unsigned char* mrow = mask + (size_t)b * N_ + s * 256;
+  for (int tile = 0; tile < 4; ++tile) {
+    {
+      const float* src = embb + (size_t)tile * 64 * D_;
+#pragma unroll
+      for (int i = 0; i < 4; ++i) {
+        const int gid = t + 256 * i;
+        const int n = gid >> 4, d0 = (gid & 15) * 8;
+        const float4 v0 = *(const float4*)(src + (size_t)n * D_ + d0);
+        const float4 v1 = *(const float4*)(src + (size_t)n * D_ + d0 + 4);
+        bf16x8 ev;
+        ev[0] = (short)bf16rne(v0.x); ev[1] = (short)bf16rne(v0.y);
+        ev[2] = (short)bf16rne(v0.z); ev[3] = (short)bf16rne(v0.w);
+        ev[4] = (short)bf16rne(v1.x); ev[5] = (short)bf16rne(v1.y);
+        ev[6] = (short)bf16rne(v1.z); ev[7] = (short)bf16rne(v1.w);
+        const int widx = ((n >> 2) * 8 + (d0 >> 4)) * 72 + ((n & 3) << 4) + (d0 & 15);
+        *(bf16x8*)&eR[widx] = ev;
+      }
+      if (t < 64) mask_s[t] = mrow[tile * 64 + t];
+    }
+    __syncthreads();
+    f32x4 sAcc = {0.f, 0.f, 0.f, 0.f};
+#pragma unroll
+    for (int ks = 0; ks < 4; ++ks) {
+      const int aidx = ((4 * w + (lc >> 2)) * 8 + 2 * ks + (lg >> 1)) * 72 +
+                       ((lc & 3) << 4) + ((lg & 1) << 3);
+      const bf16x8 af = *(const bf16x8*)&eR[aidx];
+      sAcc = __builtin_amdgcn_mfma_f32_16x16x32_bf16(af, bq[ks], sAcc, 0, 0, 0);
+    }
+    float sv[4];
+    bool mk[4];
+    float tmax = -INFINITY;
+#pragma unroll
+    for (int r = 0; r < 4; ++r) {
+      mk[r] = mask_s[16 * w + 4 * lg + r] != 0;
+      sv[r] = mk[r] ? -INFINITY : sAcc[r];
+      tmax = fmaxf(tmax, sv[r]);
+    }
+    tmax = fmaxf(tmax, __shfl_xor(tmax, 16, 64));
+    tmax = fmaxf(tmax, __shfl_xor(tmax, 32, 64));
+    if (lane < 16) red0[w * 16 + lc] = tmax;
+    __syncthreads();
+    const float m_tile = fmaxf(fmaxf(red0[lc], red0[16 + lc]),
+                               fmaxf(red0[32 + lc], red0[48 + lc]));
+    const float m_new = fmaxf(m_run, m_tile);
+    const float rsc = (m_new == -INFINITY) ? 1.f : __expf(m_run - m_new);
+    float psum = 0.f;
+    unsigned short pu[4];
+#pragma unroll
+    for (int r = 0; r < 4; ++r) {
+      const float p = mk[r] ? 0.f : __expf(sv[r] - m_new);
+      psum += p;
+      pu[r] = bf16rne(p);
+    }
+    m_run = m_new;
+    psum += __shfl_xor(psum, 16, 64);
+    psum += __shfl_xor(psum, 32, 64);
+    if (lane < 16) red1[w * 16 + lc] = psum;
+    *(u16x4*)&pT[lc * 72 + 16 * w + 4 * lg] = (u16x4){pu[0], pu[1], pu[2], pu[3]};
+    if (t < 16) resc[t] = rsc;
+    __syncthreads();
+    l_run = l_run * rsc + (red1[lc] + red1[16 + lc] + red1[32 + lc] + red1[48 + lc]);
+    {
+      const float r0f = resc[4 * lg + 0], r1f = resc[4 * lg + 1];
+      const float r2f = resc[4 * lg + 2], r3f = resc[4 * lg + 3];
+      wacc0[0] *= r0f; wacc0[1] *= r1f; wacc0[2] *= r2f; wacc0[3] *= r3f;
+      wacc1[0] *= r0f; wacc1[1] *= r1f; wacc1[2] *= r2f; wacc1[3] *= r3f;
+    }
+    i32x2 tb0a, tb0b, tb1a, tb1b, tb2a, tb2b, tb3a, tb3b;
+    {
+      const unsigned base00 = (unsigned)(unsigned long long)
+          &eR[((0 + 2 * lg) * 8 + w) * 72 + lc];
+      const unsigned base01 = (unsigned)(unsigned long long)
+          &eR[((0 + 2 * lg) * 8 + (w + 4)) * 72 + lc];
+      const unsigned base10 = (unsigned)(unsigned long long)
+          &eR[((8 + 2 * lg) * 8 + w) * 72 + lc];
+      const unsigned base11 = (unsigned)(unsigned long long)
+          &eR[((8 + 2 * lg) * 8 + (w + 4)) * 72 + lc];
+      asm volatile("ds_read_b64_tr_b16 %0, %2 offset:0\n\t"
+                   "ds_read_b64_tr_b16 %1, %2 offset:1152"
+                   : "=v"(tb0a), "=v"(tb0b) : "v"(base00));
+      asm volatile("ds_read_b64_tr_b16 %0, %2 offset:0\n\t"
+                   "ds_read_b64_tr_b16 %1, %2 offset:1152"
+                   : "=v"(tb1a), "=v"(tb1b) : "v"(base01));
+      asm volatile("ds_read_b64_tr_b16 %0, %2 offset:0\n\t"
+                   "ds_read_b64_tr_b16 %1, %2 offset:1152"
+                   : "=v"(tb2a), "=v"(tb2b) : "v"(base10));
+      asm volatile("ds_read_b64_tr_b16 %0, %2 offset:0\n\t"
+                   "ds_read_b64_tr_b16 %1, %2 offset:1152"
+                   : "=v"(tb3a), "=v"(tb3b) : "v"(base11));
+      asm volatile("s_waitcnt lgkmcnt(0)" ::: "memory");
+      __builtin_amdgcn_sched_barrier(0);
+    }
+    {
+      const bf16x8 pa0 = *(const bf16x8*)&pT[lc * 72 + 8 * lg];
+      const bf16x8 pa1 = *(const bf16x8*)&pT[lc * 72 + 32 + 8 * lg];
+      union { i32x2 d[2]; bf16x8 v; } u;
+      u.d[0] = tb0a; u.d[1] = tb0b;
+      wacc0 = __builtin_amdgcn_mfma_f32_16x16x32_bf16(pa0, u.v, wacc0, 0, 0, 0);
+      u.d[0] = tb1a; u.d[1] = tb1b;
+      wacc1 = __builtin_amdgcn_mfma_f32_16x16x32_bf16(pa0, u.v, wacc1, 0, 0, 0);
+      u.d[0] = tb2a; u.d[1] = tb2b;
+      wacc0 = __builtin_amdgcn_mfma_f32_16x16x32_bf16(pa1, u.v, wacc0, 0, 0, 0);
+      u.d[0] = tb3a; u.d[1] = tb3b;
+      wacc1 = __builtin_amdgcn_mfma_f32_16x16x32_bf16(pa1, u.v, wacc1, 0, 0, 0);
+    }
+    __syncthreads();
+  }
+  float* dst = wsA + (size_t)(b * 8 + s) * WSA_STRIDE;
+  if (lg < 2) {
+#pragma unroll
+    for (int r = 0; r < 4; ++r) {
+      const int h = 4 * lg + r;
+      dst[16 + h * 128 + 16 * w + lc] = wacc0[r];
+      dst[16 + h * 128 + 16 * (w + 4) + lc] = wacc1[r];
+    }
+  }
+  if (t < 8) { dst[t] = m_run; dst[8 + t] = l_run; }
+}
+
+__global__ void __launch_bounds__(256) k_attn_comb(const float* __restrict__ Wnode,
+                                                   const float* __restrict__ Wout,
+                                                   const float* __restrict__ wsA,
+                                                   float* __restrict__ wsC) {
+  __shared__ __align__(16) unsigned char smem[10240];
+  do_D(Wnode, Wout, wsA, wsC, blockIdx.x, threadIdx.x, smem);
 }
 
 __global__ void __launch_bounds__(256) k_logits_part(const float* __restrict__ emb,
@@ -815,15 +791,15 @@
   float* buf = (float*)d_out;
 
   int occ = 0;
-  (void)hipOccupancyMaxActiveBlocksPerMultiprocessor(&occ, k_mega, 256, 0);
+  (void)hipOccupancyMaxActiveBlocksPerMultiprocessor(&occ, k_flow, 256, 0);
 
   if (occ >= 4 && ws_size >= WS_NEED_BYTES) {
     unsigned short* wsE = (unsigned short*)d_ws;
     float* wsF = (float*)((char*)d_ws + WSE_BYTES);
-    unsigned* bar = (unsigned*)(wsF + BAR_OFF);
-    hipMemsetAsync(bar, 0, 8, stream);
-    k_mega<<<GRID_MEGA, 256, 0, stream>>>(emb, Wnode, Wfix, Wstep, Wout, fidx,
-                                          lidx, mask, buf, wsE, wsF, bar);
+    unsigned* flg = (unsigned*)(wsF + FLAGS_OFF);
+    hipMemsetAsync(flg, 0, 1280 * 4, stream);
+    k_flow<<<GRID_F, 256, 0, stream>>>(emb, Wnode, Wfix, Wstep, Wout, fidx,
+                                       lidx, mask, buf, wsE, wsF, flg);
   } else {
     float* ws = (float*)d_ws;
     k_prep<<<dim3(B_, 8), 256, 0, stream>>>(emb, buf);
```

Result: no change. 160.3 us (+0.1%).
